# Kernel tuning notes

Hardware: AMD Instinct MI355X
Metric: run time of the kernel (lower is better)

## Reference

```python
import jax, jax.numpy as jnp
import numpy as np

L = 4
B_LIST = [30, 17, 9, 5, 3]      # bandwidth schedule (geometric 30 -> 3)
F_LIST = [1, 2, 5, 12, 28, 64]  # channel schedule (geometric 1 -> 64)
BATCH = 32
C64 = jnp.complex64

# near-identity grids (beta = pi/16, 6 alphas; SO3 grid additionally 6 gammas)
_A6 = np.linspace(0.0, 2 * np.pi, 6, endpoint=False)
S2_BETA = np.full(6, np.pi / 16)
S2_ALPHA = _A6
_aa, _gg = np.meshgrid(_A6, _A6, indexing='ij')
SO3_ALPHA = _aa.ravel()
SO3_BETA = np.full(36, np.pi / 16)
SO3_GAMMA = _gg.ravel()


def betas_of(b):
    return np.pi * (2 * np.arange(2 * b) + 1) / (4 * b)


def quad_weights(b):
    j = np.arange(2 * b)
    k = np.arange(b)
    s = (np.sin(np.pi * np.outer(2 * j + 1, 2 * k + 1) / (4 * b)) / (2 * k + 1)).sum(1)
    return (2.0 / b) * np.sin(np.pi * (2 * j + 1) / (4 * b)) * s


def wigner_d_all(lmax, betas):
    """Wigner small-d d^l_{m',m}(beta) via exp(-i beta Jy); list_l of [nbeta,2l+1,2l+1]."""
    out = [np.ones((len(betas), 1, 1))]
    for l in range(1, lmax):
        m = np.arange(-l, l)
        jp = np.sqrt(l * (l + 1) - m * (m + 1))  # <m+1|J+|m>
        Jy = np.zeros((2 * l + 1, 2 * l + 1), np.complex128)
        i = np.arange(2 * l)
        Jy[i + 1, i] = -0.5j * jp
        Jy[i, i + 1] = 0.5j * jp
        lam, U = np.linalg.eigh(Jy)
        ph = np.exp(-1j * np.outer(betas, lam))
        out.append(np.einsum('ak,bk,ck->bac', U, ph, U.conj()).real)
    return out


def fft_idx(l, n):
    # indices of frequencies m = -l..l in fft ordering of length n
    return np.concatenate([np.arange(n - l, n), np.arange(l + 1)])


def s2_fft(x, b_out):
    # x: [B,f,2b,2b] real (beta,alpha) -> list_l of [B,f,2l+1] complex
    b_in = x.shape[-1] // 2
    wig = wigner_d_all(b_out, betas_of(b_in))
    w = quad_weights(b_in)
    xf = jnp.fft.fft(x, axis=-1)
    out = []
    for l in range(b_out):
        dl = jnp.asarray((wig[l][:, :, l] * w[:, None]).astype(np.complex64))  # [2b,2l+1]
        out.append(jnp.einsum('bfjm,jm->bfm', xf[..., fft_idx(l, 2 * b_in)], dl))
    return out


def so3_fft(x, b_out):
    # x: [B,f,2b,2b,2b] real (beta,alpha,gamma) -> list_l of [B,f,2l+1,2l+1]
    b_in = x.shape[-1] // 2
    wig = wigner_d_all(b_out, betas_of(b_in))
    w = quad_weights(b_in)
    xf = jnp.fft.fft2(x, axes=(-2, -1))
    out = []
    for l in range(b_out):
        idx = fft_idx(l, 2 * b_in)
        dl = jnp.asarray((wig[l] * w[:, None, None]).astype(np.complex64))
        out.append(jnp.einsum('bfjmn,jmn->bfmn', xf[:, :, :, idx[:, None], idx[None, :]], dl))
    return out


def so3_ifft(coeffs, b):
    # coeffs: list_l [B,f,2l+1,2l+1] -> real signal [B,f,2b,2b,2b]
    wig = wigner_d_all(b, betas_of(b))
    nb = 2 * b
    Bz, f = coeffs[0].shape[:2]
    X = jnp.zeros((Bz, f, nb, nb, nb), C64)
    for l in range(b):
        idx = fft_idx(l, nb)
        dl = jnp.asarray(((2 * l + 1) * wig[l]).astype(np.complex64))
        X = X.at[:, :, :, idx[:, None], idx[None, :]].add(
            jnp.einsum('bfmn,jmn->bfjmn', coeffs[l], dl))
    return (jnp.fft.ifft2(X, axes=(-2, -1)) * (nb * nb)).real


def s2_kernel_ft(k, b):
    # k: [f_in,f_out,P] -> list_l of [2l+1,f_in,f_out] complex
    wig = wigner_d_all(b, S2_BETA)
    kc = k.astype(C64)
    out = []
    for l in range(b):
        m = np.arange(-l, l + 1)
        F = (wig[l][:, :, l] * np.exp(1j * np.outer(S2_ALPHA, m))).astype(np.complex64)
        out.append(jnp.einsum('iop,pm->mio', kc, jnp.asarray(F)))
    return out


def so3_kernel_ft(k, b):
    # k: [f_in,f_out,P] -> list_l of [2l+1,2l+1,f_in,f_out] complex
    wig = wigner_d_all(b, SO3_BETA)
    kc = k.astype(C64)
    out = []
    for l in range(b):
        m = np.arange(-l, l + 1)
        F = (wig[l]
             * np.exp(1j * np.outer(SO3_ALPHA, m))[:, :, None]
             * np.exp(1j * np.outer(SO3_GAMMA, m))[:, None, :]).astype(np.complex64)
        out.append(jnp.einsum('iop,pmn->mnio', kc, jnp.asarray(F)))
    return out


def s2_conv(x, kern, b_out):
    xh = s2_fft(x, b_out)
    kh = s2_kernel_ft(kern, b_out)
    yh = [jnp.einsum('bim,nio->bomn', xh[l], kh[l].conj()) for l in range(b_out)]
    return so3_ifft(yh, b_out)


def so3_conv(x, kern, b_out):
    xh = so3_fft(x, b_out)
    kh = so3_kernel_ft(kern, b_out)
    yh = [jnp.einsum('bimk,nkio->bomn', xh[l], kh[l].conj()) for l in range(b_out)]
    return so3_ifft(yh, b_out)


def so3_integrate(x):
    b = x.shape[-1] // 2
    w = jnp.asarray(quad_weights(b).astype(np.float32))
    return jnp.einsum('bfjac,j->bf', x, w) / float((2 * b) ** 2)


def batchnorm(x, g, be):
    mu = x.mean(0)
    var = ((x - mu) ** 2).mean(0)
    return (x - mu) * jax.lax.rsqrt(var + 1e-5) * g + be


def setup_inputs() -> dict:
    key = jax.random.key(0)
    ks = jax.random.split(key, 10)
    rn = lambda k, s, sc=1.0: jax.random.normal(k, s, jnp.float32) * sc
    return {
        'x': rn(ks[0], (BATCH, 1, 60, 60)),
        'k_s2': rn(ks[1], (1, 2, 6), 0.5),
        'k1': rn(ks[2], (2, 5, 36), 0.1),
        'k2': rn(ks[3], (5, 12, 36), 0.1),
        'k3': rn(ks[4], (12, 28, 36), 0.1),
        'k4': rn(ks[5], (28, 64, 36), 0.1),
        'g1': jnp.ones(64), 'be1': jnp.zeros(64),
        'w1': rn(ks[6], (64, 64), 0.125), 'b1': jnp.zeros(64),
        'g2': jnp.ones(64), 'be2': jnp.zeros(64),
        'w2': rn(ks[7], (64, 32), 0.125), 'b2': jnp.zeros(32),
        'g3': jnp.ones(32), 'be3': jnp.zeros(32),
        'w3': rn(ks[8], (32, 10), 0.18), 'b3': jnp.zeros(10),
    }


def reference(x, k_s2, k1, k2, k3, k4, g1, be1, w1, b1, g2, be2, w2, b2, g3, be3, w3, b3):
    h = jax.nn.relu(s2_conv(x, k_s2, B_LIST[0]))            # [B,2,60,60,60]
    for k, bo in zip((k1, k2, k3, k4), B_LIST[1:]):
        h = jax.nn.relu(so3_conv(h, k, bo))                 # bandwidth shrinks 17,9,5,3
    h = so3_integrate(h)                                    # [B,64]
    h = jax.nn.relu(batchnorm(h, g1, be1) @ w1 + b1)
    h = jax.nn.relu(batchnorm(h, g2, be2) @ w2 + b2)
    return batchnorm(h, g3, be3) @ w3 + b3                  # [B,10]
```

## Files before the change

### kernel.cpp

```cpp
#include <hip/hip_runtime.h>
#include <cmath>
#include <cstring>
#include <vector>


#define DPI 3.14159265358979323846

static constexpr int OQh(int l) { return l*(4*l*l - 1)/3; }
static_assert(OQh(30) == 35990, "oq30");
static_assert(OQh(17) == 6545,  "oq17");
static_assert(OQh(9)  == 969,   "oq9");
static_assert(OQh(5)  == 165,   "oq5");
static_assert(OQh(3)  == 35,    "oq3");

static constexpr size_t WS_XF1 = 0;
static constexpr size_t WS_XH1 = WS_XF1 + 32ull*60*30*8;
static constexpr size_t WS_KH1 = WS_XH1 + 32ull*900*8;
static constexpr size_t WS_YH1 = WS_KH1 + 1800ull*8;
static constexpr size_t WS_XT2 = WS_YH1 + 64ull*35990*8;
static constexpr size_t WS_XH2 = WS_XT2 + 64ull*60*561*8;
static constexpr size_t WS_KH2 = WS_XH2 + 64ull*6545*8;
static constexpr size_t WS_YH2 = WS_KH2 + 6545ull*10*8;
static constexpr size_t WS_XT3 = WS_YH2 + 160ull*6545*8;
static constexpr size_t WS_XH3 = WS_XT3 + 160ull*34*153*8;
static constexpr size_t WS_KH3 = WS_XH3 + 160ull*969*8;
static constexpr size_t WS_YH3 = WS_KH3 + 969ull*60*8;
static constexpr size_t WS_XT4 = WS_YH3 + 384ull*969*8;
static constexpr size_t WS_XH4 = WS_XT4 + 384ull*18*45*8;
static constexpr size_t WS_KH4 = WS_XH4 + 384ull*165*8;
static constexpr size_t WS_YH4 = WS_KH4 + 165ull*336*8;
static constexpr size_t WS_XT5 = WS_YH4 + 896ull*165*8;
static constexpr size_t WS_XH5 = WS_XT5 + 896ull*10*15*8;
static constexpr size_t WS_KH5 = WS_XH5 + 896ull*35*8;
static constexpr size_t WS_YH5 = WS_KH5 + 35ull*1792*8;
static constexpr size_t WS_S5P = WS_YH5 + 2048ull*35*8;
static constexpr size_t WS_TOTAL = WS_S5P + 2048ull*6*4;

struct ConstOffs {
  size_t A1, A2, A3, A4, A5;
  size_t S1, S2, S3, S4, S5;
  size_t WInt;
  size_t nF;
  size_t Fs2, Fso3;
  size_t Tw60, Tw34, Tw18, Tw10, Tw6;
  size_t Wn1, Wn2o, Wn3, Wn4, Wn5;
  size_t Wg1, Wg2, Wg3, Wg4;
  size_t nC;
};
static ConstOffs CO;
static float*  g_devF = nullptr;
static float2* g_devC = nullptr;

static void tqli(double* d, double* e, int n, double* z) {
  e[n-1] = 0.0;
  for (int l = 0; l < n; l++) {
    int iter = 0;
    int m;
    do {
      for (m = l; m < n-1; m++) {
        double dd = fabs(d[m]) + fabs(d[m+1]);
        if (fabs(e[m]) <= 1e-300 + 1e-14*dd) break;
      }
      if (m != l) {
        if (iter++ == 80) break;
        double g = (d[l+1]-d[l])/(2.0*e[l]);
        double r = hypot(g, 1.0);
        g = d[m]-d[l]+e[l]/(g + (g >= 0.0 ? fabs(r) : -fabs(r)));
        double s = 1.0, c = 1.0, p = 0.0;
        int i;
        r = 1.0;
        for (i = m-1; i >= l; i--) {
          double f = s*e[i], b = c*e[i];
          r = hypot(f, g);
          e[i+1] = r;
          if (r == 0.0) { d[i+1] -= p; e[m] = 0.0; break; }
          s = f/r; c = g/r;
          g = d[i+1]-p;
          r = (d[i]-g)*s + 2.0*c*b;
          p = s*r;
          d[i+1] = g+p;
          g = c*r-b;
          for (int k = 0; k < n; k++) {
            f = z[(size_t)k*n+i+1];
            z[(size_t)k*n+i+1] = s*z[(size_t)k*n+i] + c*f;
            z[(size_t)k*n+i]   = c*z[(size_t)k*n+i] - s*f;
          }
        }
        if (r == 0.0 && i >= l) continue;
        d[l] -= p; e[l] = g; e[m] = 0.0;
      }
    } while (m != l);
  }
}

struct Builder {
  std::vector<std::vector<double>> V, Lam;
  bool useExpm[30];

  Builder() {
    V.resize(30); Lam.resize(30);
    for (int l = 0; l < 30; l++) {
      int n = 2*l+1;
      std::vector<double> d(n, 0.0), e(n, 0.0), z((size_t)n*n, 0.0);
      for (int i = 0; i < n; i++) z[(size_t)i*n+i] = 1.0;
      for (int i = 0; i+1 < n; i++) {
        double m = (double)i - l;
        e[i] = -0.5*sqrt((double)l*(l+1) - m*(m+1.0));
      }
      if (n > 1) tqli(d.data(), e.data(), n, z.data());
      V[l] = std::move(z); Lam[l] = std::move(d);
    }
    std::vector<double> t((size_t)59*59);
    for (int l = 0; l < 30; l++) {
      useExpm[l] = false;
      if (l == 0) continue;
      int n = 2*l+1;
      eigD(l, 0.77, t.data());
      double corner = pow(cos(0.385), 2.0*l);
      double err = fabs(t[0] - corner) + fabs(t[(size_t)(n-1)*n + (n-1)] - corner);
      double s = 0.0;
      for (int c = 0; c < n; c++) s += t[c]*t[c];
      err += fabs(s - 1.0);
      if (!(err < 1e-8)) useExpm[l] = true;
    }
  }

  void eigD(int l, double beta, double* out) {
    int n = 2*l+1;
    const double* Vp = V[l].data();
    const double* lam = Lam[l].data();
    double ck[64], sk[64];
    for (int k = 0; k < n; k++) { ck[k] = cos(beta*lam[k]); sk[k] = sin(beta*lam[k]); }
    for (int a = 0; a < n; a++) {
      const double* va = Vp + (size_t)a*n;
      for (int c = 0; c < n; c++) {
        const double* vc = Vp + (size_t)c*n;
        int r = ((a - c) % 4 + 4) % 4;
        const double* f = (r & 1) ? sk : ck;
        double s = 0.0;
        for (int k = 0; k < n; k++) s += va[k]*vc[k]*f[k];
        out[(size_t)a*n + c] = (r >= 2) ? -s : s;
      }
    }
  }

  void expmD(int l, double beta, double* out) {
    int n = 2*l+1;
    int s = 0; double bl = fabs(beta)*(double)l + 1e-12;
    while (bl > 0.25) { bl *= 0.5; s++; }
    double sc = ldexp(beta, -s);
    std::vector<double> sup(n > 1 ? n-1 : 0);
    for (int i = 0; i+1 < n; i++) {
      double m = (double)i - l;
      sup[i] = 0.5*sqrt((double)l*(l+1) - m*(m+1.0))*sc;
    }
    std::vector<double> term((size_t)n*n, 0.0), acc((size_t)n*n, 0.0), t2((size_t)n*n);
    for (int i = 0; i < n; i++) { term[(size_t)i*n+i] = 1.0; acc[(size_t)i*n+i] = 1.0; }
    for (int k = 1; k <= 16; k++) {
      for (int r = 0; r < n; r++)
        for (int c = 0; c < n; c++) {
          double v = 0.0;
          if (c > 0)   v += term[(size_t)r*n + c-1]*sup[c-1];
          if (c+1 < n) v -= term[(size_t)r*n + c+1]*sup[c];
          t2[(size_t)r*n+c] = v/(double)k;
        }
      term.swap(t2);
      for (size_t i2 = 0; i2 < (size_t)n*n; i2++) acc[i2] += term[i2];
    }
    for (int t = 0; t < s; t++) {
      for (int r = 0; r < n; r++)
        for (int c = 0; c < n; c++) {
          double v = 0.0;
          for (int k = 0; k < n; k++) v += acc[(size_t)r*n+k]*acc[(size_t)k*n+c];
          t2[(size_t)r*n+c] = v;
        }
      acc.swap(t2);
    }
    std::memcpy(out, acc.data(), sizeof(double)*(size_t)n*n);
  }

  void buildD(int l, double beta, double* out) {
    if (useExpm[l]) expmD(l, beta, out); else eigD(l, beta, out);
  }
};

static std::vector<double> quadw_h(int b) {
  std::vector<double> w(2*b);
  for (int j = 0; j < 2*b; j++) {
    double s = 0;
    for (int k = 0; k < b; k++)
      s += sin(DPI*(2*j+1)*(2*k+1)/(4.0*b))/(double)(2*k+1);
    w[j] = (2.0/b)*sin(DPI*(2*j+1)/(4.0*b))*s;
  }
  return w;
}

static void build_all() {
  size_t o = 0;
  CO.A1 = o; o += 60ull*900;
  CO.A2 = o; o += 60ull*OQh(17);
  CO.A3 = o; o += 34ull*OQh(9);
  CO.A4 = o; o += 18ull*OQh(5);
  CO.A5 = o; o += 10ull*OQh(3);
  CO.S1 = o; o += 60ull*OQh(30);
  CO.S2 = o; o += 34ull*OQh(17);
  CO.S3 = o; o += 18ull*OQh(9);
  CO.S4 = o; o += 10ull*OQh(5);
  CO.S5 = o; o +=  6ull*OQh(3);
  CO.WInt = o; o += 8;
  CO.nF = o;
  size_t c = 0;
  CO.Fs2  = c; c += 6ull*900;
  CO.Fso3 = c; c += 36ull*OQh(17);
  CO.Tw60 = c; c += 60; CO.Tw34 = c; c += 34; CO.Tw18 = c; c += 18;
  CO.Tw10 = c; c += 10; CO.Tw6  = c; c += 6;
  CO.Wn1 = c; c += 30*60; CO.Wn2o = c; c += 17*34; CO.Wn3 = c; c += 9*18;
  CO.Wn4 = c; c += 5*10;  CO.Wn5 = c; c += 3*6;
  CO.Wg1 = c; c += 60*17; CO.Wg2 = c; c += 34*9; CO.Wg3 = c; c += 18*5;
  CO.Wg4 = c; c += 10*3;
  CO.nC = c;

  std::vector<float> HF(CO.nF, 0.f);
  std::vector<float> HC(2*CO.nC, 0.f);

  Builder B;
  auto betas = [](int b){ std::vector<double> v(2*b);
    for (int j = 0; j < 2*b; j++) v[j] = DPI*(2*j+1)/(4.0*b); return v; };
  auto w30 = quadw_h(30), w17 = quadw_h(17), w9 = quadw_h(9), w5 = quadw_h(5), w3 = quadw_h(3);
  std::vector<double> tmp((size_t)59*59);

  { auto bs = betas(30);
    for (int l = 0; l < 30; l++) { int n = 2*l+1;
      for (int j = 0; j < 60; j++) {
        B.buildD(l, bs[j], tmp.data());
        float* dst = HF.data() + CO.S1 + 60ull*OQh(l) + (size_t)j*n*n;
        for (int i2 = 0; i2 < n*n; i2++) dst[i2] = (float)((2*l+1)*tmp[i2]);
        if (l < 17) {
          float* dA = HF.data() + CO.A2 + 60ull*OQh(l) + (size_t)j*n*n;
          for (int i2 = 0; i2 < n*n; i2++) dA[i2] = (float)(tmp[i2]*w30[j]);
        }
        float* dA1 = HF.data() + CO.A1 + 60ull*l*l + (size_t)j*n;
        for (int mi = 0; mi < n; mi++) dA1[mi] = (float)(tmp[(size_t)mi*n + l]*w30[j]);
      } } }
  { auto bs = betas(17);
    for (int l = 0; l < 17; l++) { int n = 2*l+1;
      for (int j = 0; j < 34; j++) {
        B.buildD(l, bs[j], tmp.data());
        float* dst = HF.data() + CO.S2 + 34ull*OQh(l) + (size_t)j*n*n;
        for (int i2 = 0; i2 < n*n; i2++) dst[i2] = (float)((2*l+1)*tmp[i2]);
        if (l < 9) {
          float* dA = HF.data() + CO.A3 + 34ull*OQh(l) + (size_t)j*n*n;
          for (int i2 = 0; i2 < n*n; i2++) dA[i2] = (float)(tmp[i2]*w17[j]);
        } } } }
  { auto bs = betas(9);
    for (int l = 0; l < 9; l++) { int n = 2*l+1;
      for (int j = 0; j < 18; j++) {
        B.buildD(l, bs[j], tmp.data());
        float* dst = HF.data() + CO.S3 + 18ull*OQh(l) + (size_t)j*n*n;
        for (int i2 = 0; i2 < n*n; i2++) dst[i2] = (float)((2*l+1)*tmp[i2]);
        if (l < 5) {
          float* dA = HF.data() + CO.A4 + 18ull*OQh(l) + (size_t)j*n*n;
          for (int i2 = 0; i2 < n*n; i2++) dA[i2] = (float)(tmp[i2]*w9[j]);
        } } } }
  { auto bs = betas(5);
    for (int l = 0; l < 5; l++) { int n = 2*l+1;
      for (int j = 0; j < 10; j++) {
        B.buildD(l, bs[j], tmp.data());
        float* dst = HF.data() + CO.S4 + 10ull*OQh(l) + (size_t)j*n*n;
        for (int i2 = 0; i2 < n*n; i2++) dst[i2] = (float)((2*l+1)*tmp[i2]);
        if (l < 3) {
          float* dA = HF.data() + CO.A5 + 10ull*OQh(l) + (size_t)j*n*n;
          for (int i2 = 0; i2 < n*n; i2++) dA[i2] = (float)(tmp[i2]*w5[j]);
        } } } }
  { auto bs = betas(3);
    for (int l = 0; l < 3; l++) { int n = 2*l+1;
      for (int j = 0; j < 6; j++) {
        B.buildD(l, bs[j], tmp.data());
        float* dst = HF.data() + CO.S5 + 6ull*OQh(l) + (size_t)j*n*n;
        for (int i2 = 0; i2 < n*n; i2++) dst[i2] = (float)((2*l+1)*tmp[i2]);
      } } }
  { double beta = DPI/16.0;
    for (int l = 0; l < 30; l++) { int n = 2*l+1;
      B.buildD(l, beta, tmp.data());
      for (int p = 0; p < 6; p++) {
        double al = 2.0*DPI*p/6.0;
        for (int mi = 0; mi < n; mi++) {
          double ph = al*(double)(mi - l);
          double dr = tmp[(size_t)mi*n + l];
          size_t off = CO.Fs2 + 6ull*l*l + (size_t)p*n + mi;
          HC[2*off]   = (float)(dr*cos(ph));
          HC[2*off+1] = (float)(dr*sin(ph));
        } }
      if (l < 17) {
        for (int p = 0; p < 36; p++) {
          double al = 2.0*DPI*(p/6)/6.0, ga = 2.0*DPI*(p%6)/6.0;
          for (int mi = 0; mi < n; mi++)
            for (int ni = 0; ni < n; ni++) {
              double ph = al*(double)(mi - l) + ga*(double)(ni - l);
              double dr = tmp[(size_t)mi*n + ni];
              size_t off = CO.Fso3 + 36ull*OQh(l) + (size_t)p*n*n + (size_t)mi*n + ni;
              HC[2*off]   = (float)(dr*cos(ph));
              HC[2*off+1] = (float)(dr*sin(ph));
            } } } } }
  auto fillTw = [&](size_t ofs, int N){
    for (int t = 0; t < N; t++) {
      HC[2*(ofs+t)]   = (float)cos(2.0*DPI*t/N);
      HC[2*(ofs+t)+1] = (float)sin(2.0*DPI*t/N);
    } };
  fillTw(CO.Tw60, 60); fillTw(CO.Tw34, 34); fillTw(CO.Tw18, 18);
  fillTw(CO.Tw10, 10); fillTw(CO.Tw6, 6);
  auto fillWn = [&](size_t ofs, int BQ, int N){
    for (int n = 0; n < BQ; n++)
      for (int cc2 = 0; cc2 < N; cc2++) {
        double f = (n == 0) ? 1.0 : 2.0;
        HC[2*(ofs + (size_t)n*N + cc2)]   = (float)(f*cos(2.0*DPI*n*cc2/N));
        HC[2*(ofs + (size_t)n*N + cc2)+1] = (float)(f*sin(2.0*DPI*n*cc2/N));
      } };
  auto fillWg = [&](size_t ofs, int N, int KT){
    for (int cc2 = 0; cc2 < N; cc2++)
      for (int k = 0; k < KT; k++) {
        HC[2*(ofs + (size_t)cc2*KT + k)]   = (float)cos(2.0*DPI*k*cc2/N);
        HC[2*(ofs + (size_t)cc2*KT + k)+1] = (float)(-sin(2.0*DPI*k*cc2/N));
      } };
  fillWn(CO.Wn1, 30, 60); fillWn(CO.Wn2o, 17, 34); fillWn(CO.Wn3, 9, 18);
  fillWn(CO.Wn4, 5, 10);  fillWn(CO.Wn5, 3, 6);
  fillWg(CO.Wg1, 60, 17); fillWg(CO.Wg2, 34, 9); fillWg(CO.Wg3, 18, 5);
  fillWg(CO.Wg4, 10, 3);
  for (int j = 0; j < 6; j++) HF[CO.WInt + j] = (float)(w3[j]/36.0);

  size_t fb = CO.nF * sizeof(float);
  size_t fbA = (fb + 255) & ~(size_t)255;
  size_t cb = CO.nC * sizeof(float2);
  void* base = nullptr;
  if (hipMalloc(&base, fbA + cb) != hipSuccess || !base) return;
  if (hipMemcpy(base, HF.data(), fb, hipMemcpyHostToDevice) != hipSuccess) return;
  if (hipMemcpy((char*)base + fbA, HC.data(), cb, hipMemcpyHostToDevice) != hipSuccess) return;
  (void)hipDeviceSynchronize();
  g_devF = (float*)base;
  g_devC = (float2*)((char*)base + fbA);
}
namespace { struct InitOnce { InitOnce(){ build_all(); } } g_once; }

__device__ __forceinline__ int OQ(int l) { return l*(4*l*l - 1)/3; }
__device__ __forceinline__ int lFromQ(int q, int L) {
  int l = 0;
  while (l+1 < L && OQ(l+1) <= q) l++;
  return l;
}
__device__ __forceinline__ int lsq(int q) {
  int l = (int)sqrtf((float)q);
  while ((l+1)*(l+1) <= q) l++;
  while (l*l > q) l--;
  return l;
}
__device__ __forceinline__ void rotf(float2& r, float2 s) {
  float t = r.x*s.x - r.y*s.y;
  r.y = r.x*s.y + r.y*s.x;
  r.x = t;
}

__global__ __launch_bounds__(256) void k_kh_s2(
    const float* __restrict__ ks2, const float2* __restrict__ F, float2* __restrict__ kh)
{
  int id = blockIdx.x*blockDim.x + threadIdx.x;
  if (id >= 1800) return;
  int q = id >> 1, o = id & 1;
  int l = lsq(q); int W = 2*l+1; int mi = q - l*l;
  const float2* Fb = F + 6ull*l*l;
  float ax = 0.f, ay = 0.f;
  for (int p = 0; p < 6; p++) {
    float kv = ks2[o*6 + p];
    float2 f = Fb[p*W + mi];
    ax += kv*f.x; ay += kv*f.y;
  }
  kh[(size_t)q*2 + o] = make_float2(ax, ay);
}

__global__ __launch_bounds__(256) void k_kh_so3(
    const float* __restrict__ kk, const float2* __restrict__ F,
    float2* __restrict__ kh, int L, int fi, int fo)
{
  int id = blockIdx.x*blockDim.x + threadIdx.x;
  int ff = fi*fo;
  if (id >= OQ(L)*ff) return;
  int q = id / ff, r = id - q*ff;
  int i = r / fo, o = r - i*fo;
  int l = lFromQ(q, L); int W = 2*l+1; int W21 = W*W;
  int rem = q - OQ(l);
  const float2* Fb = F + 36ull*OQ(l) + rem;
  const float* kb = kk + (size_t)(i*fo + o)*36;
  float ax = 0.f, ay = 0.f;
  for (int p = 0; p < 36; p++) {
    float kv = kb[p];
    float2 f = Fb[(size_t)p*W21];
    ax += kv*f.x; ay += kv*f.y;
  }
  kh[(size_t)q*ff + r] = make_float2(ax, ay);
}

__global__ __launch_bounds__(64) void k_s1_fftA(
    const float* __restrict__ x, const float2* __restrict__ tw, float2* __restrict__ XF1)
{
  __shared__ float row[60];
  int b = blockIdx.x / 60, j = blockIdx.x - b*60;
  int t = threadIdx.x;
  if (t < 60) row[t] = x[((size_t)b*60 + j)*60 + t];
  __syncthreads();
  if (t < 30) {
    float ax = 0.f, ay = 0.f;
    int ti = 0;
    for (int a = 0; a < 60; a++) {
      float2 w = tw[ti];
      ax += row[a]*w.x; ay -= row[a]*w.y;
      ti += t; if (ti >= 60) ti -= 60;
    }
    XF1[((size_t)b*60 + j)*30 + t] = make_float2(ax, ay);
  }
}

__global__ __launch_bounds__(256) void k_s1_coef(
    const float2* __restrict__ XF1, const float* __restrict__ dA1, float2* __restrict__ xh1)
{
  int id = blockIdx.x*blockDim.x + threadIdx.x;
  if (id >= 32*900) return;
  int b = id / 900, q = id - b*900;
  int l = lsq(q); int W = 2*l+1; int mi = q - l*l; int m = mi - l;
  const float* dp = dA1 + 60ull*l*l + mi;
  const float2* xb = XF1 + (size_t)b*60*30;
  int ma = m >= 0 ? m : -m;
  float sg = m >= 0 ? 1.f : -1.f;
  float ax = 0.f, ay = 0.f;
  for (int j = 0; j < 60; j++) {
    float2 xf = xb[j*30 + ma];
    float d = dp[(size_t)j*W];
    ax += d*xf.x; ay += sg*d*xf.y;
  }
  xh1[id] = make_float2(ax, ay);
}

__global__ __launch_bounds__(256) void k_s1_yh(
    const float2* __restrict__ xh1, const float2* __restrict__ kh1, float2* __restrict__ yh1)
{
  int id = blockIdx.x*blockDim.x + threadIdx.x;
  if (id >= 64*35990) return;
  int bo = id / 35990, q = id - bo*35990;
  int b = bo >> 1, o = bo & 1;
  int l = lFromQ(q, 30); int W = 2*l+1;
  int rem = q - OQ(l); int mi = rem / W, ni = rem - mi*W;
  float2 xv = xh1[(size_t)b*900 + l*l + mi];
  float2 kv = kh1[(size_t)(l*l + ni)*2 + o];
  yh1[id] = make_float2(xv.x*kv.x + xv.y*kv.y, xv.y*kv.x - xv.x*kv.y);
}

__global__ __launch_bounds__(256) void k_yh(
    const float2* __restrict__ xh, const float2* __restrict__ kh,
    float2* __restrict__ yh, int L, int fi, int fo, int Qtot)
{
  int id = blockIdx.x*blockDim.x + threadIdx.x;
  if (id >= 32*fo*Qtot) return;
  int bo = id / Qtot, q = id - bo*Qtot;
  int b = bo / fo, o = bo - b*fo;
  int l = lFromQ(q, L); int W = 2*l+1;
  int rem = q - OQ(l); int mi = rem / W, ni = rem - mi*W;
  int ff = fi*fo;
  const float2* xb = xh + ((size_t)b*fi)*Qtot + OQ(l) + mi*W;
  const float2* kb = kh + ((size_t)(OQ(l) + ni*W))*ff + o;
  float ax = 0.f, ay = 0.f;
  for (int i = 0; i < fi; i++) {
    const float2* xrow = xb + (size_t)i*Qtot;
    const float2* krow = kb + (size_t)i*fo;
    for (int k = 0; k < W; k++) {
      float2 xv = xrow[k];
      float2 kv = krow[(size_t)k*ff];
      ax += xv.x*kv.x + xv.y*kv.y;
      ay += xv.y*kv.x - xv.x*kv.y;
    }
  }
  yh[id] = make_float2(ax, ay);
}

__global__ __launch_bounds__(256) void k_coef(
    const float2* __restrict__ xt, const float* __restrict__ dA,
    float2* __restrict__ xh, int L, int nj, int KT, int MT, int Qtot, int nbi)
{
  int id = blockIdx.x*blockDim.x + threadIdx.x;
  if (id >= nbi*Qtot) return;
  int bi = id / Qtot, q = id - bi*Qtot;
  int l = lFromQ(q, L); int W = 2*l+1; int W21 = W*W;
  int rem = q - OQ(l); int mi = rem / W, ki = rem - mi*W;
  int m = mi - l, ks = ki - l;
  const float* dAp = dA + (size_t)nj*OQ(l) + rem;
  int MTKT = MT*KT;
  int pidx; float sgn;
  if (ks >= 0) { pidx = (m + (KT-1))*KT + ks;  sgn =  1.f; }
  else         { pidx = (-m + (KT-1))*KT - ks; sgn = -1.f; }
  const float2* xb = xt + (size_t)bi*nj*MTKT + pidx;
  float ax = 0.f, ay = 0.f;
  for (int j = 0; j < nj; j++) {
    float2 xv = xb[(size_t)j*MTKT];
    float d = dAp[(size_t)j*W21];
    ax += d*xv.x; ay += sgn*d*xv.y;
  }
  xh[id] = make_float2(ax, ay);
}

template<int BQ, int N, int KT, int MT, int TPB>
__global__ __launch_bounds__(TPB) void k_synth3(
    const float2* __restrict__ yh, const float* __restrict__ dS,
    const float2* __restrict__ twN, float2* __restrict__ xt)
{
  constexpr int W2  = 2*BQ - 1;
  constexpr int NH  = N/2;
  constexpr int CP  = (BQ+3) & ~3;
  constexpr int KTP = (KT+1) & ~1;
  constexpr int QT  = BQ*(4*BQ*BQ - 1)/3;
  constexpr int R3  = (N%4 == 0) ? 4 : 2;
  constexpr int RP  = (NH%2 == 0) ? 2 : 1;
  constexpr int SZA0 = (W2*CP*8 > 2*N*NH*4) ? W2*CP*8 : 2*N*NH*4;
  constexpr int SZA  = (SZA0 + 15) & ~15;
  constexpr int SZB0 = (N*CP*8 > 2*NH*KTP*8) ? N*CP*8 : 2*NH*KTP*8;
  constexpr int SZB  = (SZB0 + 15) & ~15;
  __shared__ __align__(16) char smem[SZA + SZB + N*8];
  float2* P   = (float2*)smem;
  float*  SS  = (float*)smem;
  float*  SD  = SS + N*NH;
  float2* Tm  = (float2*)(smem + SZA);
  float2* USS = (float2*)(smem + SZA);
  float2* USD = USS + NH*KTP;
  float2* twl = (float2*)(smem + SZA + SZB);

  const int tid = threadIdx.x;
  int nwg = gridDim.x, bidx = blockIdx.x;
  int per = nwg >> 3;
  int swz = (bidx & 7)*per + (bidx >> 3);
  int bo = swz / N, j = swz - bo*N;

  for (int t = tid; t < N; t += TPB) twl[t] = twN[t];

  const float2* yhb = yh + (size_t)bo*QT;
  for (int idx = tid; idx < W2*CP; idx += TPB) {
    int pm = idx / CP, n = idx - pm*CP;
    float ax = 0.f, ay = 0.f;
    if (n < BQ) {
      int m = pm - (BQ-1);
      int am = m < 0 ? -m : m;
      int lmin = am > n ? am : n;
      int base = lmin*(4*lmin*lmin - 1)/3;
      for (int l = lmin; l < BQ; l++) {
        int Wl = 2*l+1;
        float2 y = yhb[base + (m+l)*Wl + (n+l)];
        float d = dS[(size_t)N*base + (size_t)j*Wl*Wl + (m+l)*Wl + (n+l)];
        ax += d*y.x; ay += d*y.y;
        base += Wl*Wl;
      }
    }
    P[idx] = make_float2(ax, ay);
  }
  __syncthreads();

  {
    constexpr int CG = CP/4;
    constexpr float SGN = ((BQ-1) & 1) ? -1.f : 1.f;
    const float4* P4 = (const float4*)P;
    for (int it = tid; it < NH*CG; it += TPB) {
      int a = it / CG, cg = it - a*CG;
      float2 s2 = twl[2*a];
      float2 r = make_float2(1.f, 0.f);
      float4 E0 = {0,0,0,0}, E1 = {0,0,0,0}, O0 = {0,0,0,0}, O1 = {0,0,0,0};
      for (int jj = 0; jj < BQ-1; jj++) {
        float4 e0 = P4[(2*jj)*(CP/2) + 2*cg];
        float4 e1 = P4[(2*jj)*(CP/2) + 2*cg + 1];
        float4 o0 = P4[(2*jj+1)*(CP/2) + 2*cg];
        float4 o1 = P4[(2*jj+1)*(CP/2) + 2*cg + 1];
        E0.x += e0.x*r.x - e0.y*r.y; E0.y += e0.x*r.y + e0.y*r.x;
        E0.z += e0.z*r.x - e0.w*r.y; E0.w += e0.z*r.y + e0.w*r.x;
        E1.x += e1.x*r.x - e1.y*r.y; E1.y += e1.x*r.y + e1.y*r.x;
        E1.z += e1.z*r.x - e1.w*r.y; E1.w += e1.z*r.y + e1.w*r.x;
        O0.x += o0.x*r.x - o0.y*r.y; O0.y += o0.x*r.y + o0.y*r.x;
        O0.z += o0.z*r.x - o0.w*r.y; O0.w += o0.z*r.y + o0.w*r.x;
        O1.x += o1.x*r.x - o1.y*r.y; O1.y += o1.x*r.y + o1.y*r.x;
        O1.z += o1.z*r.x - o1.w*r.y; O1.w += o1.z*r.y + o1.w*r.x;
        rotf(r, s2);
      }
      {
        float4 e0 = P4[(2*(BQ-1))*(CP/2) + 2*cg];
        float4 e1 = P4[(2*(BQ-1))*(CP/2) + 2*cg + 1];
        E0.x += e0.x*r.x - e0.y*r.y; E0.y += e0.x*r.y + e0.y*r.x;
        E0.z += e0.z*r.x - e0.w*r.y; E0.w += e0.z*r.y + e0.w*r.x;
        E1.x += e1.x*r.x - e1.y*r.y; E1.y += e1.x*r.y + e1.y*r.x;
        E1.z += e1.z*r.x - e1.w*r.y; E1.w += e1.z*r.y + e1.w*r.x;
      }
      float2 wa = twl[a];
      int pidx = (N - (a*(BQ-1)) % N) % N;
      float2 ph = twl[pidx];
      int c0 = 4*cg;
      auto doCol = [&](float ex, float ey, float ox, float oy, int col) {
        float gx = ox*wa.x - oy*wa.y, gy = ox*wa.y + oy*wa.x;
        float px = ex + gx, py = ey + gy;
        float qx = ex - gx, qy = ey - gy;
        Tm[a*CP + col]        = make_float2(px*ph.x - py*ph.y, px*ph.y + py*ph.x);
        Tm[(a+NH)*CP + col]   = make_float2(SGN*(qx*ph.x - qy*ph.y), SGN*(qx*ph.y + qy*ph.x));
      };
      doCol(E0.x, E0.y, O0.x, O0.y, c0+0);
      doCol(E0.z, E0.w, O0.z, O0.w, c0+1);
      doCol(E1.x, E1.y, O1.x, O1.y, c0+2);
      doCol(E1.z, E1.w, O1.z, O1.w, c0+3);
    }
  }
  __syncthreads();

  {
    constexpr int NO3 = BQ/2;
    constexpr int NRG = N/R3;
    for (int it = tid; it < NRG*NH; it += TPB) {
      int rg = it / NH, c = it - rg*NH;
      int a0 = rg*R3;
      float2 se = twl[2*c];
      float2 re = make_float2(1.f, 0.f);
      float2 ro = twl[c];
      float er[R3], orr[R3];
      #pragma unroll
      for (int rr = 0; rr < R3; rr++) { er[rr] = 0.f; orr[rr] = 0.f; }
      for (int jj = 0; jj < NO3; jj++) {
        #pragma unroll
        for (int rr = 0; rr < R3; rr++) {
          float4 tv = *(const float4*)&Tm[(a0+rr)*CP + 2*jj];
          er[rr]  += tv.x*re.x - tv.y*re.y;
          orr[rr] += tv.z*ro.x - tv.w*ro.y;
        }
        rotf(re, se); rotf(ro, se);
      }
      if constexpr ((BQ & 1) != 0) {
        #pragma unroll
        for (int rr = 0; rr < R3; rr++) {
          float2 tv = Tm[(a0+rr)*CP + (BQ-1)];
          er[rr] += tv.x*re.x - tv.y*re.y;
        }
      }
      #pragma unroll
      for (int rr = 0; rr < R3; rr++) {
        float t0x = Tm[(a0+rr)*CP].x;
        float s0 = fmaxf(2.f*(er[rr] + orr[rr]) - t0x, 0.f);
        float s1 = fmaxf(2.f*(er[rr] - orr[rr]) - t0x, 0.f);
        SS[(a0+rr)*NH + c] = s0 + s1;
        SD[(a0+rr)*NH + c] = s0 - s1;
      }
    }
  }
  __syncthreads();

  {
    for (int it = tid; it < (NH/RP)*KT; it += TPB) {
      int g = it / KT, k = it - g*KT;
      int a0 = g*RP;
      const float* Sp = (k & 1) ? SD : SS;
      float2 st = twl[k]; st.y = -st.y;
      float2 r = make_float2(1.f, 0.f);
      float ux[2*RP], uy[2*RP];
      #pragma unroll
      for (int q2 = 0; q2 < 2*RP; q2++) { ux[q2] = 0.f; uy[q2] = 0.f; }
      for (int c = 0; c < NH; c++) {
        #pragma unroll
        for (int pp = 0; pp < RP; pp++) {
          float sl = Sp[(a0+pp)*NH + c];
          float sh = Sp[(a0+pp+NH)*NH + c];
          ux[2*pp]   += sl*r.x; uy[2*pp]   += sl*r.y;
          ux[2*pp+1] += sh*r.x; uy[2*pp+1] += sh*r.y;
        }
        rotf(r, st);
      }
      #pragma unroll
      for (int pp = 0; pp < RP; pp++) {
        USS[(a0+pp)*KTP + k] = make_float2(ux[2*pp] + ux[2*pp+1], uy[2*pp] + uy[2*pp+1]);
        USD[(a0+pp)*KTP + k] = make_float2(ux[2*pp] - ux[2*pp+1], uy[2*pp] - uy[2*pp+1]);
      }
    }
  }
  __syncthreads();

  {
    float2* xtb = xt + ((size_t)bo*N + j)*(MT*KT);
    constexpr int KG = KTP/2;
    for (int it = tid; it < MT*KG; it += TPB) {
      int pm2 = it / KG, kg = it - pm2*KG;
      int m = pm2 - (KT-1);
      int mm = m < 0 ? m + N : m;
      const float2* Up = (m & 1) ? USD : USS;
      float2 st = twl[mm];
      float2 r = make_float2(1.f, 0.f);
      float a0x = 0.f, a0y = 0.f, a1x = 0.f, a1y = 0.f;
      for (int a = 0; a < NH; a++) {
        float4 u = *(const float4*)&Up[a*KTP + 2*kg];
        a0x += u.x*r.x + u.y*r.y;  a0y += u.y*r.x - u.x*r.y;
        a1x += u.z*r.x + u.w*r.y;  a1y += u.w*r.x - u.z*r.y;
        rotf(r, st);
      }
      int k0 = 2*kg;
      xtb[pm2*KT + k0] = make_float2(a0x, a0y);
      if (k0 + 1 < KT) xtb[pm2*KT + k0 + 1] = make_float2(a1x, a1y);
    }
  }
}

template<int BQ, int N, int KT, int MT, int INTEG, int NPAIR, int TPB>
__global__ __launch_bounds__(TPB) void k_synth2(
    const float2* __restrict__ yh, const float* __restrict__ dS,
    const float2* __restrict__ twN, const float2* __restrict__ Wn2,
    const float2* __restrict__ Wg, float2* __restrict__ xt,
    float* __restrict__ s5p, const float* __restrict__ wInt)
{
  constexpr int W2 = 2*BQ - 1;
  constexpr int QT = BQ*(4*BQ*BQ - 1)/3;
  constexpr int SZA = (((W2*BQ*8 > N*N*4) ? W2*BQ*8 : N*N*4) + 15) & ~15;
  constexpr int SZB0 = (N*BQ*8 > N*KT*8) ? N*BQ*8 : N*KT*8;
  constexpr int SZB1 = (SZB0 > TPB*4) ? SZB0 : TPB*4;
  constexpr int SZB = (SZB1 + 15) & ~15;
  __shared__ __align__(16) char smem[SZA + SZB + N*8];
  float2* P   = (float2*)smem;
  float*  S   = (float*)smem;
  float2* Tm  = (float2*)(smem + SZA);
  float2* U   = (float2*)(smem + SZA);
  float*  red = (float*)(smem + SZA);
  float2* twl = (float2*)(smem + SZA + SZB);

  const int tid = threadIdx.x;
  int bidx = blockIdx.x, nwg = gridDim.x;
  int per = nwg >> 3;
  int swz = (bidx & 7)*per + (bidx >> 3);
  int bo = swz / N, j = swz - bo*N;

  for (int t = tid; t < N; t += TPB) twl[t] = twN[t];
  __syncthreads();

  const float2* yhb = yh + (size_t)bo*QT;
  for (int idx = tid; idx < W2*BQ; idx += TPB) {
    int pm = idx / BQ, n = idx - pm*BQ;
    int m = pm - (BQ-1);
    int am = m < 0 ? -m : m;
    int lmin = am > n ? am : n;
    int base = lmin*(4*lmin*lmin - 1)/3;
    float ax = 0.f, ay = 0.f;
    for (int l = lmin; l < BQ; l++) {
      int Wl = 2*l+1;
      float2 y = yhb[base + (m+l)*Wl + (n+l)];
      float d = dS[(size_t)N*base + (size_t)j*Wl*Wl + (m+l)*Wl + (n+l)];
      ax += d*y.x; ay += d*y.y;
      base += Wl*Wl;
    }
    P[idx] = make_float2(ax, ay);
  }
  __syncthreads();

  for (int idx = tid; idx < (N/2)*BQ; idx += TPB) {
    int ag = idx / BQ, n = idx - ag*BQ;
    int a0 = 2*ag, a1 = a0 + 1;
    int t0 = (N - (a0*(BQ-1)) % N) % N;
    int t1 = (N - (a1*(BQ-1)) % N) % N;
    float2 A0 = {0,0}, A1 = {0,0};
    for (int pm = 0; pm < W2; pm++) {
      float2 p = P[pm*BQ + n];
      float2 w0 = twl[t0], w1 = twl[t1];
      A0.x += p.x*w0.x - p.y*w0.y; A0.y += p.x*w0.y + p.y*w0.x;
      A1.x += p.x*w1.x - p.y*w1.y; A1.y += p.x*w1.y + p.y*w1.x;
      t0 += a0; if (t0 >= N) t0 -= N;
      t1 += a1; if (t1 >= N) t1 -= N;
    }
    Tm[a0*BQ + n] = A0;
    Tm[a1*BQ + n] = A1;
  }
  __syncthreads();

  {
    constexpr int CG = N/2;
    const float4* WnR = (const float4*)Wn2;
    for (int idx = tid; idx < N*CG; idx += TPB) {
      int a = idx / CG, cg = idx - a*CG;
      float s0 = 0.f, s1 = 0.f;
      const float2* TmA = Tm + a*BQ;
      for (int n = 0; n < BQ; n++) {
        float2 T = TmA[n];
        float4 w = WnR[n*CG + cg];
        s0 += T.x*w.x - T.y*w.y;
        s1 += T.x*w.z - T.y*w.w;
      }
      s0 = fmaxf(s0, 0.f); s1 = fmaxf(s1, 0.f);
      *(float2*)&S[a*N + 2*cg] = make_float2(s0, s1);
    }
  }
  __syncthreads();

  if constexpr (!INTEG) {
    for (int idx = tid; idx < (N/2)*KT; idx += TPB) {
      int ag = idx / KT, k = idx - ag*KT;
      int a0 = 2*ag, a1 = a0 + 1;
      float u0x=0.f,u0y=0.f,u1x=0.f,u1y=0.f;
      const float* S0 = S + a0*N;
      const float* S1 = S + a1*N;
      for (int c = 0; c < N; c++) {
        float2 w = Wg[c*KT + k];
        u0x += S0[c]*w.x; u0y += S0[c]*w.y;
        u1x += S1[c]*w.x; u1y += S1[c]*w.y;
      }
      U[a0*KT + k] = make_float2(u0x, u0y);
      U[a1*KT + k] = make_float2(u1x, u1y);
    }
    __syncthreads();

    float2* xtb = xt + ((size_t)bo*N + j)*(MT*KT);
    for (int idx = tid; idx < MT*KT; idx += TPB) {
      int pm2 = idx / KT, k = idx - pm2*KT;
      int m = pm2 - (KT-1);
      float ax = 0.f, ay = 0.f;
      int t = 0;
      for (int a = 0; a < N; a++) {
        float2 u = U[a*KT + k];
        float2 w = twl[t];
        ax += u.x*w.x + u.y*w.y;
        ay += u.y*w.x - u.x*w.y;
        t += m; if (t < 0) t += N; else if (t >= N) t -= N;
      }
      xtb[idx] = make_float2(ax, ay);
    }
  } else {
    float part = 0.f;
    for (int idx = tid; idx < N*N; idx += TPB) part += S[idx];
    red[tid] = part;
    __syncthreads();
    for (int off2 = TPB >> 1; off2 > 0; off2 >>= 1) {
      if (tid < off2) red[tid] += red[tid + off2];
      __syncthreads();
    }
    if (tid == 0) s5p[bo*N + j] = red[0]*wInt[j];
  }
}

__global__ __launch_bounds__(256) void k_mlp(
    const float* __restrict__ s5p,
    const float* __restrict__ g1, const float* __restrict__ be1,
    const float* __restrict__ w1, const float* __restrict__ b1,
    const float* __restrict__ g2, const float* __restrict__ be2,
    const float* __restrict__ w2, const float* __restrict__ b2,
    const float* __restrict__ g3, const float* __restrict__ be3,
    const float* __restrict__ w3, const float* __restrict__ b3,
    float* __restrict__ out)
{
  __shared__ float A[2048], Bs[2048], C[1024], mu[64], iv[64];
  int tid = threadIdx.x;
  for (int idx = tid; idx < 2048; idx += 256) {
    float s = 0.f;
    #pragma unroll
    for (int j = 0; j < 6; j++) s += s5p[idx*6 + j];
    A[idx] = s;
  }
  __syncthreads();
  if (tid < 64) {
    float m = 0.f; for (int b = 0; b < 32; b++) m += A[b*64 + tid]; m *= (1.f/32);
    float v = 0.f; for (int b = 0; b < 32; b++) { float d = A[b*64+tid]-m; v += d*d; } v *= (1.f/32);
    mu[tid] = m; iv[tid] = rsqrtf(v + 1e-5f)*g1[tid];
  }
  __syncthreads();
  for (int idx = tid; idx < 2048; idx += 256) {
    int f = idx & 63;
    A[idx] = (A[idx]-mu[f])*iv[f] + be1[f];
  }
  __syncthreads();
  for (int idx = tid; idx < 2048; idx += 256) {
    int b = idx >> 6, fo = idx & 63;
    float s = b1[fo];
    for (int f = 0; f < 64; f++) s += A[b*64+f]*w1[f*64+fo];
    Bs[idx] = fmaxf(s, 0.f);
  }
  __syncthreads();
  if (tid < 64) {
    float m = 0.f; for (int b = 0; b < 32; b++) m += Bs[b*64+tid]; m *= (1.f/32);
    float v = 0.f; for (int b = 0; b < 32; b++) { float d = Bs[b*64+tid]-m; v += d*d; } v *= (1.f/32);
    mu[tid] = m; iv[tid] = rsqrtf(v + 1e-5f)*g2[tid];
  }
  __syncthreads();
  for (int idx = tid; idx < 2048; idx += 256) {
    int f = idx & 63;
    Bs[idx] = (Bs[idx]-mu[f])*iv[f] + be2[f];
  }
  __syncthreads();
  for (int idx = tid; idx < 1024; idx += 256) {
    int b = idx >> 5, fo = idx & 31;
    float s = b2[fo];
    for (int f = 0; f < 64; f++) s += Bs[b*64+f]*w2[f*32+fo];
    C[idx] = fmaxf(s, 0.f);
  }
  __syncthreads();
  if (tid < 32) {
    float m = 0.f; for (int b = 0; b < 32; b++) m += C[b*32+tid]; m *= (1.f/32);
    float v = 0.f; for (int b = 0; b < 32; b++) { float d = C[b*32+tid]-m; v += d*d; } v *= (1.f/32);
    mu[tid] = m; iv[tid] = rsqrtf(v + 1e-5f)*g3[tid];
  }
  __syncthreads();
  for (int idx = tid; idx < 1024; idx += 256) {
    int f = idx & 31;
    C[idx] = (C[idx]-mu[f])*iv[f] + be3[f];
  }
  __syncthreads();
  for (int idx = tid; idx < 320; idx += 256) {
    int b = idx/10, cc = idx - b*10;
    float s = b3[cc];
    for (int f = 0; f < 32; f++) s += C[b*32+f]*w3[f*10+cc];
    out[idx] = s;
  }
}

static inline int cdiv_h(int a, int b) { return (a + b - 1)/b; }

extern "C" void kernel_launch(void* const* d_in, const int* in_sizes, int n_in,
                              void* d_out, int out_size, void* d_ws, size_t ws_size,
                              hipStream_t stream) {
  (void)in_sizes; (void)n_in; (void)out_size;
  if (!g_devF || !g_devC || ws_size < WS_TOTAL) return;

  const float* x    = (const float*)d_in[0];
  const float* ks2  = (const float*)d_in[1];
  const float* k1   = (const float*)d_in[2];
  const float* k2   = (const float*)d_in[3];
  const float* k3   = (const float*)d_in[4];
  const float* k4   = (const float*)d_in[5];
  const float* g1   = (const float*)d_in[6],  *be1 = (const float*)d_in[7];
  const float* w1   = (const float*)d_in[8],  *b1  = (const float*)d_in[9];
  const float* g2   = (const float*)d_in[10], *be2 = (const float*)d_in[11];
  const float* w2   = (const float*)d_in[12], *b2  = (const float*)d_in[13];
  const float* g3   = (const float*)d_in[14], *be3 = (const float*)d_in[15];
  const float* w3   = (const float*)d_in[16], *b3  = (const float*)d_in[17];
  float* out = (float*)d_out;
  char* ws = (char*)d_ws;

  float2* XF1 = (float2*)(ws + WS_XF1);
  float2* xh1 = (float2*)(ws + WS_XH1);
  float2* kh1 = (float2*)(ws + WS_KH1);
  float2* yh1 = (float2*)(ws + WS_YH1);
  float2* xt2 = (float2*)(ws + WS_XT2);
  float2* xh2 = (float2*)(ws + WS_XH2);
  float2* kh2 = (float2*)(ws + WS_KH2);
  float2* yh2 = (float2*)(ws + WS_YH2);
  float2* xt3 = (float2*)(ws + WS_XT3);
  float2* xh3 = (float2*)(ws + WS_XH3);
  float2* kh3 = (float2*)(ws + WS_KH3);
  float2* yh3 = (float2*)(ws + WS_YH3);
  float2* xt4 = (float2*)(ws + WS_XT4);
  float2* xh4 = (float2*)(ws + WS_XH4);
  float2* kh4 = (float2*)(ws + WS_KH4);
  float2* yh4 = (float2*)(ws + WS_YH4);
  float2* xt5 = (float2*)(ws + WS_XT5);
  float2* xh5 = (float2*)(ws + WS_XH5);
  float2* kh5 = (float2*)(ws + WS_KH5);
  float2* yh5 = (float2*)(ws + WS_YH5);
  float*  s5p = (float*) (ws + WS_S5P);

  const float* dA1p = g_devF + CO.A1; const float* dA2p = g_devF + CO.A2;
  const float* dA3p = g_devF + CO.A3; const float* dA4p = g_devF + CO.A4;
  const float* dA5p = g_devF + CO.A5;
  const float* dS1p = g_devF + CO.S1; const float* dS2p = g_devF + CO.S2;
  const float* dS3p = g_devF + CO.S3; const float* dS4p = g_devF + CO.S4;
  const float* dS5p = g_devF + CO.S5;
  const float* wIntp = g_devF + CO.WInt;
  const float2* Fs2p  = g_devC + CO.Fs2;
  const float2* Fso3p = g_devC + CO.Fso3;
  const float2* tw60p = g_devC + CO.Tw60; const float2* tw34p = g_devC + CO.Tw34;
  const float2* tw18p = g_devC + CO.Tw18; const float2* tw10p = g_devC + CO.Tw10;
  const float2* tw6p  = g_devC + CO.Tw6;
  const float2* Wn4p = g_devC + CO.Wn4; const float2* Wn5p = g_devC + CO.Wn5;
  const float2* Wg4p = g_devC + CO.Wg4;

  constexpr int Q30 = OQh(30), Q17 = OQh(17), Q9 = OQh(9), Q5 = OQh(5), Q3 = OQh(3);

  k_kh_s2 <<<cdiv_h(1800,256),      256, 0, stream>>>(ks2, Fs2p,  kh1);
  k_kh_so3<<<cdiv_h(Q17*10,256),    256, 0, stream>>>(k1, Fso3p, kh2, 17, 2, 5);
  k_kh_so3<<<cdiv_h(Q9*60,256),     256, 0, stream>>>(k2, Fso3p, kh3, 9, 5, 12);
  k_kh_so3<<<cdiv_h(Q5*336,256),    256, 0, stream>>>(k3, Fso3p, kh4, 5, 12, 28);
  k_kh_so3<<<cdiv_h(Q3*1792,256),   256, 0, stream>>>(k4, Fso3p, kh5, 3, 28, 64);

  k_s1_fftA<<<32*60, 64, 0, stream>>>(x, tw60p, XF1);
  k_s1_coef<<<cdiv_h(32*900,256), 256, 0, stream>>>(XF1, dA1p, xh1);
  k_s1_yh  <<<cdiv_h(64*Q30,256), 256, 0, stream>>>(xh1, kh1, yh1);

  k_synth3<30,60,17,33,256><<<64*60,  256, 0, stream>>>(yh1, dS1p, tw60p, xt2);
  k_coef <<<cdiv_h(64*Q17,256),  256, 0, stream>>>(xt2, dA2p, xh2, 17, 60, 17, 33, Q17, 64);
  k_yh   <<<cdiv_h(160*Q17,256), 256, 0, stream>>>(xh2, kh2, yh2, 17, 2, 5, Q17);

  k_synth3<17,34,9,17,128><<<160*34, 128, 0, stream>>>(yh2, dS2p, tw34p, xt3);
  k_coef <<<cdiv_h(160*Q9,256),  256, 0, stream>>>(xt3, dA3p, xh3, 9, 34, 9, 17, Q9, 160);
  k_yh   <<<cdiv_h(384*Q9,256),  256, 0, stream>>>(xh3, kh3, yh3, 9, 5, 12, Q9);

  k_synth3<9,18,5,9,64><<<384*18, 64, 0, stream>>>(yh3, dS3p, tw18p, xt4);
  k_coef <<<cdiv_h(384*Q5,256),  256, 0, stream>>>(xt4, dA4p, xh4, 5, 18, 5, 9, Q5, 384);
  k_yh   <<<cdiv_h(896*Q5,256),  256, 0, stream>>>(xh4, kh4, yh4, 5, 12, 28, Q5);

  k_synth2<5,10,3,5,0,1,64><<<896*10, 64, 0, stream>>>(yh4, dS4p, tw10p, Wn4p, Wg4p, xt5, nullptr, nullptr);
  k_coef <<<cdiv_h(896*Q3,256),  256, 0, stream>>>(xt5, dA5p, xh5, 3, 10, 3, 5, Q3, 896);
  k_yh   <<<cdiv_h(2048*Q3,256), 256, 0, stream>>>(xh5, kh5, yh5, 3, 28, 64, Q3);

  k_synth2<3,6,3,5,1,1,64><<<2048*6, 64, 0, stream>>>(yh5, dS5p, tw6p, Wn5p, nullptr, nullptr, s5p, wIntp);

  k_mlp<<<1, 256, 0, stream>>>(s5p, g1, be1, w1, b1, g2, be2, w2, b2, g3, be3, w3, b3, out);
}
```

Measured before the change: 936.4 us.

## Restructure SO(3) inverse transforms into scatter plus staged DFT GEMM passes

Replaces the fused per-beta synthesis kernels for the two largest SO(3) stages with a scatter kernel that exploits Wigner-d symmetry (only n>=0 terms, packed per (m,n) with precomputed offsets), followed by separable DFT passes over alpha and gamma done as small matrix products in chunks. The spectral intermediates are transposed so batch/channel is innermost, which gives coalesced access, and the forward coefficient kernels read transposed beta-major Wigner tables and use the Hermitian half-spectrum. This is meant to cut the redundant work and uncoalesced reads in the large synthesis steps. In exchange it adds more launches and large scratch buffers, and the index bookkeeping is more intricate.

```diff
diff --git a/kernel.cpp b/kernel.cpp
--- a/kernel.cpp
+++ b/kernel.cpp
@@ -2,6 +2,7 @@
 #include <cmath>
 #include <cstring>
 #include <vector>
+#include <algorithm>
 
 
 #define DPI 3.14159265358979323846
@@ -13,43 +14,52 @@
 static_assert(OQh(5)  == 165,   "oq5");
 static_assert(OQh(3)  == 35,    "oq3");
 
-static constexpr size_t WS_XF1 = 0;
-static constexpr size_t WS_XH1 = WS_XF1 + 32ull*60*30*8;
-static constexpr size_t WS_KH1 = WS_XH1 + 32ull*900*8;
-static constexpr size_t WS_YH1 = WS_KH1 + 1800ull*8;
-static constexpr size_t WS_XT2 = WS_YH1 + 64ull*35990*8;
-static constexpr size_t WS_XH2 = WS_XT2 + 64ull*60*561*8;
-static constexpr size_t WS_KH2 = WS_XH2 + 64ull*6545*8;
-static constexpr size_t WS_YH2 = WS_KH2 + 6545ull*10*8;
-static constexpr size_t WS_XT3 = WS_YH2 + 160ull*6545*8;
-static constexpr size_t WS_XH3 = WS_XT3 + 160ull*34*153*8;
-static constexpr size_t WS_KH3 = WS_XH3 + 160ull*969*8;
-static constexpr size_t WS_YH3 = WS_KH3 + 969ull*60*8;
-static constexpr size_t WS_XT4 = WS_YH3 + 384ull*969*8;
-static constexpr size_t WS_XH4 = WS_XT4 + 384ull*18*45*8;
-static constexpr size_t WS_KH4 = WS_XH4 + 384ull*165*8;
-static constexpr size_t WS_YH4 = WS_KH4 + 165ull*336*8;
-static constexpr size_t WS_XT5 = WS_YH4 + 896ull*165*8;
-static constexpr size_t WS_XH5 = WS_XT5 + 896ull*10*15*8;
-static constexpr size_t WS_KH5 = WS_XH5 + 896ull*35*8;
-static constexpr size_t WS_YH5 = WS_KH5 + 35ull*1792*8;
-static constexpr size_t WS_S5P = WS_YH5 + 2048ull*35*8;
-static constexpr size_t WS_TOTAL = WS_S5P + 2048ull*6*4;
+static constexpr int T1SUM = 18445;
+static constexpr int T2SUM = 3417;
+
+static constexpr size_t al256(size_t x){ return (x + 255) & ~(size_t)255; }
+static constexpr size_t WS_XF1  = 0;
+static constexpr size_t WS_XH1  = WS_XF1  + al256(32ull*60*30*8);
+static constexpr size_t WS_KH1  = WS_XH1  + al256(32ull*900*8);
+static constexpr size_t WS_YH1T = WS_KH1  + al256(1800ull*8);
+static constexpr size_t WS_XH2  = WS_YH1T + al256(35990ull*64*8);
+static constexpr size_t WS_KH2  = WS_XH2  + al256(64ull*6545*8);
+static constexpr size_t WS_YH2T = WS_KH2  + al256(6545ull*10*8);
+static constexpr size_t WS_XH3  = WS_YH2T + al256(6545ull*160*8);
+static constexpr size_t WS_KH3  = WS_XH3  + al256(160ull*969*8);
+static constexpr size_t WS_YH3T = WS_KH3  + al256(969ull*60*8);
+static constexpr size_t WS_XT4  = WS_YH3T + al256(969ull*384*8);
+static constexpr size_t WS_XH4  = WS_XT4  + al256(384ull*18*45*8);
+static constexpr size_t WS_KH4  = WS_XH4  + al256(384ull*165*8);
+static constexpr size_t WS_YH4T = WS_KH4  + al256(165ull*336*8);
+static constexpr size_t WS_XT5  = WS_YH4T + al256(165ull*896*8);
+static constexpr size_t WS_XH5  = WS_XT5  + al256(896ull*10*15*8);
+static constexpr size_t WS_KH5  = WS_XH5  + al256(896ull*35*8);
+static constexpr size_t WS_YH5T = WS_KH5  + al256(35ull*1792*8);
+static constexpr size_t WS_S5P  = WS_YH5T + al256(35ull*2048*8);
+static constexpr size_t WS_XT2  = WS_S5P  + al256(2048ull*6*4);
+static constexpr size_t WS_XT3  = WS_XT2  + al256(561ull*3840*8);
+static constexpr size_t WS_RX   = WS_XT3  + al256(153ull*5440*8);
+static constexpr size_t WS_RY   = WS_RX   + al256(1770ull*960*8);
+static constexpr size_t WS_TOTAL= WS_RY   + al256(1728000ull*8);
 
 struct ConstOffs {
-  size_t A1, A2, A3, A4, A5;
-  size_t S1, S2, S3, S4, S5;
+  size_t A1, dAT2, dAT3, A4, A5;
+  size_t dT1, dT2;
+  size_t S3, S4, S5;
   size_t WInt;
   size_t nF;
   size_t Fs2, Fso3;
-  size_t Tw60, Tw34, Tw18, Tw10, Tw6;
-  size_t Wn1, Wn2o, Wn3, Wn4, Wn5;
-  size_t Wg1, Wg2, Wg3, Wg4;
+  size_t Tw60, Tw18, Tw10, Tw6;
+  size_t Wn1, Wn2o, Wn4, Wn5;
+  size_t Wg1, Wg2, Wg4;
+  size_t WA1t, WA2t, WC1, WC2;
   size_t nC;
 };
 static ConstOffs CO;
 static float*  g_devF = nullptr;
 static float2* g_devC = nullptr;
+static int*    g_devI = nullptr;
 
 static void tqli(double* d, double* e, int n, double* z) {
   e[n-1] = 0.0;
@@ -197,31 +207,47 @@
 
 static void build_all() {
   size_t o = 0;
-  CO.A1 = o; o += 60ull*900;
-  CO.A2 = o; o += 60ull*OQh(17);
-  CO.A3 = o; o += 34ull*OQh(9);
-  CO.A4 = o; o += 18ull*OQh(5);
-  CO.A5 = o; o += 10ull*OQh(3);
-  CO.S1 = o; o += 60ull*OQh(30);
-  CO.S2 = o; o += 34ull*OQh(17);
-  CO.S3 = o; o += 18ull*OQh(9);
-  CO.S4 = o; o += 10ull*OQh(5);
-  CO.S5 = o; o +=  6ull*OQh(3);
+  CO.A1   = o; o += 60ull*900;
+  CO.dAT2 = o; o += (size_t)OQh(17)*60;
+  CO.dAT3 = o; o += (size_t)OQh(9)*34;
+  CO.A4   = o; o += 18ull*OQh(5);
+  CO.A5   = o; o += 10ull*OQh(3);
+  CO.dT1  = o; o += (size_t)T1SUM*60;
+  CO.dT2  = o; o += (size_t)T2SUM*34;
+  CO.S3   = o; o += 18ull*OQh(9);
+  CO.S4   = o; o += 10ull*OQh(5);
+  CO.S5   = o; o +=  6ull*OQh(3);
   CO.WInt = o; o += 8;
   CO.nF = o;
   size_t c = 0;
   CO.Fs2  = c; c += 6ull*900;
   CO.Fso3 = c; c += 36ull*OQh(17);
-  CO.Tw60 = c; c += 60; CO.Tw34 = c; c += 34; CO.Tw18 = c; c += 18;
-  CO.Tw10 = c; c += 10; CO.Tw6  = c; c += 6;
-  CO.Wn1 = c; c += 30*60; CO.Wn2o = c; c += 17*34; CO.Wn3 = c; c += 9*18;
-  CO.Wn4 = c; c += 5*10;  CO.Wn5 = c; c += 3*6;
-  CO.Wg1 = c; c += 60*17; CO.Wg2 = c; c += 34*9; CO.Wg3 = c; c += 18*5;
-  CO.Wg4 = c; c += 10*3;
+  CO.Tw60 = c; c += 60; CO.Tw18 = c; c += 18; CO.Tw10 = c; c += 10; CO.Tw6 = c; c += 6;
+  CO.Wn1  = c; c += 30*60; CO.Wn2o = c; c += 17*34;
+  CO.Wn4  = c; c += 5*10;  CO.Wn5  = c; c += 3*6;
+  CO.Wg1  = c; c += 60*17; CO.Wg2  = c; c += 34*9; CO.Wg4 = c; c += 10*3;
+  CO.WA1t = c; c += 59*60;
+  CO.WA2t = c; c += 33*34;
+  CO.WC1  = c; c += 33*60;
+  CO.WC2  = c; c += 17*34;
   CO.nC = c;
 
   std::vector<float> HF(CO.nF, 0.f);
   std::vector<float> HC(2*CO.nC, 0.f);
+
+  std::vector<int> HI(1770 + 561);
+  { int acc = 0;
+    for (int pm = 0; pm < 59; pm++) for (int n = 0; n < 30; n++) {
+      int m = pm - 29, am = m < 0 ? -m : m;
+      int lm = am > n ? am : n;
+      HI[pm*30 + n] = acc; acc += 30 - lm;
+    } }
+  { int acc = 0;
+    for (int pm = 0; pm < 33; pm++) for (int n = 0; n < 17; n++) {
+      int m = pm - 16, am = m < 0 ? -m : m;
+      int lm = am > n ? am : n;
+      HI[1770 + pm*17 + n] = acc; acc += 17 - lm;
+    } }
 
   Builder B;
   auto betas = [](int b){ std::vector<double> v(2*b);
@@ -230,54 +256,66 @@
   std::vector<double> tmp((size_t)59*59);
 
   { auto bs = betas(30);
-    for (int l = 0; l < 30; l++) { int n = 2*l+1;
+    for (int l = 0; l < 30; l++) { int W = 2*l+1;
       for (int j = 0; j < 60; j++) {
         B.buildD(l, bs[j], tmp.data());
-        float* dst = HF.data() + CO.S1 + 60ull*OQh(l) + (size_t)j*n*n;
-        for (int i2 = 0; i2 < n*n; i2++) dst[i2] = (float)((2*l+1)*tmp[i2]);
+        for (int mm = -l; mm <= l; mm++)
+          for (int nn = 0; nn <= l; nn++) {
+            int am = mm < 0 ? -mm : mm;
+            int lmin = am > nn ? am : nn;
+            int term = HI[(mm+29)*30 + nn] + (l - lmin);
+            HF[CO.dT1 + (size_t)term*60 + j] =
+              (float)((2*l+1)*tmp[(size_t)(mm+l)*W + (nn+l)]);
+          }
         if (l < 17) {
-          float* dA = HF.data() + CO.A2 + 60ull*OQh(l) + (size_t)j*n*n;
-          for (int i2 = 0; i2 < n*n; i2++) dA[i2] = (float)(tmp[i2]*w30[j]);
+          for (int rem = 0; rem < W*W; rem++)
+            HF[CO.dAT2 + (size_t)(OQh(l)+rem)*60 + j] = (float)(tmp[rem]*w30[j]);
         }
-        float* dA1 = HF.data() + CO.A1 + 60ull*l*l + (size_t)j*n;
-        for (int mi = 0; mi < n; mi++) dA1[mi] = (float)(tmp[(size_t)mi*n + l]*w30[j]);
+        float* dA1 = HF.data() + CO.A1 + 60ull*l*l + (size_t)j*W;
+        for (int mi = 0; mi < W; mi++) dA1[mi] = (float)(tmp[(size_t)mi*W + l]*w30[j]);
       } } }
   { auto bs = betas(17);
-    for (int l = 0; l < 17; l++) { int n = 2*l+1;
+    for (int l = 0; l < 17; l++) { int W = 2*l+1;
       for (int j = 0; j < 34; j++) {
         B.buildD(l, bs[j], tmp.data());
-        float* dst = HF.data() + CO.S2 + 34ull*OQh(l) + (size_t)j*n*n;
-        for (int i2 = 0; i2 < n*n; i2++) dst[i2] = (float)((2*l+1)*tmp[i2]);
+        for (int mm = -l; mm <= l; mm++)
+          for (int nn = 0; nn <= l; nn++) {
+            int am = mm < 0 ? -mm : mm;
+            int lmin = am > nn ? am : nn;
+            int term = HI[1770 + (mm+16)*17 + nn] + (l - lmin);
+            HF[CO.dT2 + (size_t)term*34 + j] =
+              (float)((2*l+1)*tmp[(size_t)(mm+l)*W + (nn+l)]);
+          }
         if (l < 9) {
-          float* dA = HF.data() + CO.A3 + 34ull*OQh(l) + (size_t)j*n*n;
-          for (int i2 = 0; i2 < n*n; i2++) dA[i2] = (float)(tmp[i2]*w17[j]);
+          for (int rem = 0; rem < W*W; rem++)
+            HF[CO.dAT3 + (size_t)(OQh(l)+rem)*34 + j] = (float)(tmp[rem]*w17[j]);
         } } } }
   { auto bs = betas(9);
-    for (int l = 0; l < 9; l++) { int n = 2*l+1;
+    for (int l = 0; l < 9; l++) { int W = 2*l+1;
       for (int j = 0; j < 18; j++) {
         B.buildD(l, bs[j], tmp.data());
-        float* dst = HF.data() + CO.S3 + 18ull*OQh(l) + (size_t)j*n*n;
-        for (int i2 = 0; i2 < n*n; i2++) dst[i2] = (float)((2*l+1)*tmp[i2]);
+        float* dst = HF.data() + CO.S3 + 18ull*OQh(l) + (size_t)j*W*W;
+        for (int i2 = 0; i2 < W*W; i2++) dst[i2] = (float)((2*l+1)*tmp[i2]);
         if (l < 5) {
-          float* dA = HF.data() + CO.A4 + 18ull*OQh(l) + (size_t)j*n*n;
-          for (int i2 = 0; i2 < n*n; i2++) dA[i2] = (float)(tmp[i2]*w9[j]);
+          float* dA = HF.data() + CO.A4 + 18ull*OQh(l) + (size_t)j*W*W;
+          for (int i2 = 0; i2 < W*W; i2++) dA[i2] = (float)(tmp[i2]*w9[j]);
         } } } }
   { auto bs = betas(5);
-    for (int l = 0; l < 5; l++) { int n = 2*l+1;
+    for (int l = 0; l < 5; l++) { int W = 2*l+1;
       for (int j = 0; j < 10; j++) {
         B.buildD(l, bs[j], tmp.data());
-        float* dst = HF.data() + CO.S4 + 10ull*OQh(l) + (size_t)j*n*n;
-        for (int i2 = 0; i2 < n*n; i2++) dst[i2] = (float)((2*l+1)*tmp[i2]);
+        float* dst = HF.data() + CO.S4 + 10ull*OQh(l) + (size_t)j*W*W;
+        for (int i2 = 0; i2 < W*W; i2++) dst[i2] = (float)((2*l+1)*tmp[i2]);
         if (l < 3) {
-          float* dA = HF.data() + CO.A5 + 10ull*OQh(l) + (size_t)j*n*n;
-          for (int i2 = 0; i2 < n*n; i2++) dA[i2] = (float)(tmp[i2]*w5[j]);
+          float* dA = HF.data() + CO.A5 + 10ull*OQh(l) + (size_t)j*W*W;
+          for (int i2 = 0; i2 < W*W; i2++) dA[i2] = (float)(tmp[i2]*w5[j]);
         } } } }
   { auto bs = betas(3);
-    for (int l = 0; l < 3; l++) { int n = 2*l+1;
+    for (int l = 0; l < 3; l++) { int W = 2*l+1;
       for (int j = 0; j < 6; j++) {
         B.buildD(l, bs[j], tmp.data());
-        float* dst = HF.data() + CO.S5 + 6ull*OQh(l) + (size_t)j*n*n;
-        for (int i2 = 0; i2 < n*n; i2++) dst[i2] = (float)((2*l+1)*tmp[i2]);
+        float* dst = HF.data() + CO.S5 + 6ull*OQh(l) + (size_t)j*W*W;
+        for (int i2 = 0; i2 < W*W; i2++) dst[i2] = (float)((2*l+1)*tmp[i2]);
       } } }
   { double beta = DPI/16.0;
     for (int l = 0; l < 30; l++) { int n = 2*l+1;
@@ -307,8 +345,7 @@
       HC[2*(ofs+t)]   = (float)cos(2.0*DPI*t/N);
       HC[2*(ofs+t)+1] = (float)sin(2.0*DPI*t/N);
     } };
-  fillTw(CO.Tw60, 60); fillTw(CO.Tw34, 34); fillTw(CO.Tw18, 18);
-  fillTw(CO.Tw10, 10); fillTw(CO.Tw6, 6);
+  fillTw(CO.Tw60, 60); fillTw(CO.Tw18, 18); fillTw(CO.Tw10, 10); fillTw(CO.Tw6, 6);
   auto fillWn = [&](size_t ofs, int BQ, int N){
     for (int n = 0; n < BQ; n++)
       for (int cc2 = 0; cc2 < N; cc2++) {
@@ -322,22 +359,49 @@
         HC[2*(ofs + (size_t)cc2*KT + k)]   = (float)cos(2.0*DPI*k*cc2/N);
         HC[2*(ofs + (size_t)cc2*KT + k)+1] = (float)(-sin(2.0*DPI*k*cc2/N));
       } };
-  fillWn(CO.Wn1, 30, 60); fillWn(CO.Wn2o, 17, 34); fillWn(CO.Wn3, 9, 18);
+  fillWn(CO.Wn1, 30, 60); fillWn(CO.Wn2o, 17, 34);
   fillWn(CO.Wn4, 5, 10);  fillWn(CO.Wn5, 3, 6);
-  fillWg(CO.Wg1, 60, 17); fillWg(CO.Wg2, 34, 9); fillWg(CO.Wg3, 18, 5);
-  fillWg(CO.Wg4, 10, 3);
+  fillWg(CO.Wg1, 60, 17); fillWg(CO.Wg2, 34, 9); fillWg(CO.Wg4, 10, 3);
+  for (int pm = 0; pm < 59; pm++)
+    for (int a = 0; a < 60; a++) {
+      double th = 2.0*DPI*a*(pm-29)/60.0;
+      HC[2*(CO.WA1t + (size_t)pm*60 + a)]   = (float)cos(th);
+      HC[2*(CO.WA1t + (size_t)pm*60 + a)+1] = (float)sin(th);
+    }
+  for (int pm = 0; pm < 33; pm++)
+    for (int a = 0; a < 34; a++) {
+      double th = 2.0*DPI*a*(pm-16)/34.0;
+      HC[2*(CO.WA2t + (size_t)pm*34 + a)]   = (float)cos(th);
+      HC[2*(CO.WA2t + (size_t)pm*34 + a)+1] = (float)sin(th);
+    }
+  for (int p = 0; p < 33; p++)
+    for (int a = 0; a < 60; a++) {
+      double th = 2.0*DPI*(p-16)*a/60.0;
+      HC[2*(CO.WC1 + (size_t)p*60 + a)]   = (float)cos(th);
+      HC[2*(CO.WC1 + (size_t)p*60 + a)+1] = (float)sin(th);
+    }
+  for (int p = 0; p < 17; p++)
+    for (int a = 0; a < 34; a++) {
+      double th = 2.0*DPI*(p-8)*a/34.0;
+      HC[2*(CO.WC2 + (size_t)p*34 + a)]   = (float)cos(th);
+      HC[2*(CO.WC2 + (size_t)p*34 + a)+1] = (float)sin(th);
+    }
   for (int j = 0; j < 6; j++) HF[CO.WInt + j] = (float)(w3[j]/36.0);
 
-  size_t fb = CO.nF * sizeof(float);
-  size_t fbA = (fb + 255) & ~(size_t)255;
-  size_t cb = CO.nC * sizeof(float2);
+  size_t fb  = CO.nF * sizeof(float);
+  size_t fbA = al256(fb);
+  size_t cb  = CO.nC * sizeof(float2);
+  size_t cbA = al256(cb);
+  size_t ib  = HI.size() * sizeof(int);
   void* base = nullptr;
-  if (hipMalloc(&base, fbA + cb) != hipSuccess || !base) return;
+  if (hipMalloc(&base, fbA + cbA + ib) != hipSuccess || !base) return;
   if (hipMemcpy(base, HF.data(), fb, hipMemcpyHostToDevice) != hipSuccess) return;
   if (hipMemcpy((char*)base + fbA, HC.data(), cb, hipMemcpyHostToDevice) != hipSuccess) return;
+  if (hipMemcpy((char*)base + fbA + cbA, HI.data(), ib, hipMemcpyHostToDevice) != hipSuccess) return;
   (void)hipDeviceSynchronize();
   g_devF = (float*)base;
   g_devC = (float2*)((char*)base + fbA);
+  g_devI = (int*)((char*)base + fbA + cbA);
 }
 namespace { struct InitOnce { InitOnce(){ build_all(); } } g_once; }
 
@@ -438,27 +502,28 @@
   xh1[id] = make_float2(ax, ay);
 }
 
-__global__ __launch_bounds__(256) void k_s1_yh(
-    const float2* __restrict__ xh1, const float2* __restrict__ kh1, float2* __restrict__ yh1)
-{
-  int id = blockIdx.x*blockDim.x + threadIdx.x;
-  if (id >= 64*35990) return;
-  int bo = id / 35990, q = id - bo*35990;
+__global__ __launch_bounds__(256) void k_s1_yh_t(
+    const float2* __restrict__ xh1, const float2* __restrict__ kh1, float2* __restrict__ yht)
+{
+  int id = blockIdx.x*256 + threadIdx.x;
+  if (id >= 35990*64) return;
+  int q = id >> 6, bo = id & 63;
   int b = bo >> 1, o = bo & 1;
   int l = lFromQ(q, 30); int W = 2*l+1;
   int rem = q - OQ(l); int mi = rem / W, ni = rem - mi*W;
   float2 xv = xh1[(size_t)b*900 + l*l + mi];
   float2 kv = kh1[(size_t)(l*l + ni)*2 + o];
-  yh1[id] = make_float2(xv.x*kv.x + xv.y*kv.y, xv.y*kv.x - xv.x*kv.y);
-}
-
-__global__ __launch_bounds__(256) void k_yh(
+  yht[id] = make_float2(xv.x*kv.x + xv.y*kv.y, xv.y*kv.x - xv.x*kv.y);
+}
+
+__global__ __launch_bounds__(256) void k_yh_t(
     const float2* __restrict__ xh, const float2* __restrict__ kh,
-    float2* __restrict__ yh, int L, int fi, int fo, int Qtot)
-{
-  int id = blockIdx.x*blockDim.x + threadIdx.x;
-  if (id >= 32*fo*Qtot) return;
-  int bo = id / Qtot, q = id - bo*Qtot;
+    float2* __restrict__ yht, int L, int fi, int fo, int Qtot)
+{
+  int id = blockIdx.x*256 + threadIdx.x;
+  int BOF = 32*fo;
+  if (id >= Qtot*BOF) return;
+  int q = id / BOF, bo = id - q*BOF;
   int b = bo / fo, o = bo - b*fo;
   int l = lFromQ(q, L); int W = 2*l+1;
   int rem = q - OQ(l); int mi = rem / W, ni = rem - mi*W;
@@ -476,7 +541,34 @@
       ay += xv.y*kv.x - xv.x*kv.y;
     }
   }
-  yh[id] = make_float2(ax, ay);
+  yht[id] = make_float2(ax, ay);
+}
+
+template<int L, int NJ, int KT, int TPB>
+__global__ __launch_bounds__(TPB) void k_coef_t(
+    const float2* __restrict__ xtN, const float* __restrict__ dAT,
+    float2* __restrict__ xh, int Qtot, int nbi, int SLfull)
+{
+  int id = blockIdx.x*TPB + threadIdx.x;
+  if (id >= nbi*Qtot) return;
+  int bi = id / Qtot, q = id - bi*Qtot;
+  int l = lFromQ(q, L); int W = 2*l+1;
+  int rem = q - OQ(l); int mi = rem / W, ki = rem - mi*W;
+  int m = mi - l, ks = ki - l;
+  int pidx; float sgn;
+  if (ks >= 0) { pidx = (m + (KT-1))*KT + ks;  sgn =  1.f; }
+  else         { pidx = (-m + (KT-1))*KT - ks; sgn = -1.f; }
+  const float2* xb = xtN + (size_t)pidx*SLfull + (size_t)bi*NJ;
+  const float* dp = dAT + (size_t)q*NJ;
+  float ax = 0.f, ay = 0.f;
+  #pragma unroll 4
+  for (int j = 0; j < NJ; j += 2) {
+    float2 d2 = *(const float2*)&dp[j];
+    float2 xa = xb[j], xc = xb[j+1];
+    ax += d2.x*xa.x + d2.y*xc.x;
+    ay += d2.x*xa.y + d2.y*xc.y;
+  }
+  xh[id] = make_float2(ax, sgn*ay);
 }
 
 __global__ __launch_bounds__(256) void k_coef(
@@ -504,7 +596,158 @@
   xh[id] = make_float2(ax, ay);
 }
 
-template<int BQ, int N, int KT, int MT, int TPB>
+
+template<int BQ, int NJ, int BOC, int TPB>
+__global__ __launch_bounds__(TPB) void k_scat(
+    const float2* __restrict__ yht, const float* __restrict__ dT,
+    const int* __restrict__ toff, float2* __restrict__ P,
+    int boLo, int BO)
+{
+  constexpr int CH = BOC*NJ;
+  __shared__ float2 Ys[BQ*BOC];
+  __shared__ float  Ds[BQ*NJ];
+  const int mn = blockIdx.x;
+  const int pm = mn / BQ, n = mn - pm*BQ;
+  const int m = pm - (BQ-1);
+  const int am = m < 0 ? -m : m;
+  const int lmin = am > n ? am : n;
+  const int K = BQ - lmin;
+  const int tof = toff[mn];
+  for (int idx = threadIdx.x; idx < K*BOC; idx += TPB) {
+    int kk = idx / BOC, bo = idx - kk*BOC;
+    int l = lmin + kk;
+    int q = OQ(l) + (m+l)*(2*l+1) + (n+l);
+    Ys[idx] = yht[(size_t)q*BO + boLo + bo];
+  }
+  for (int idx = threadIdx.x; idx < K*NJ; idx += TPB)
+    Ds[idx] = dT[(size_t)tof*NJ + idx];
+  __syncthreads();
+  float2* Pb = P + (size_t)mn*CH;
+  for (int o = threadIdx.x; o < CH; o += TPB) {
+    int bo = o / NJ, j = o - bo*NJ;
+    float ax = 0.f, ay = 0.f;
+    for (int kk = 0; kk < K; kk++) {
+      float2 y = Ys[kk*BOC + bo];
+      float d = Ds[kk*NJ + j];
+      ax = fmaf(d, y.x, ax); ay = fmaf(d, y.y, ay);
+    }
+    Pb[o] = make_float2(ax, ay);
+  }
+}
+
+template<int NPM, int NN, int AROWS, int NAH, int NAT, int CHSL, int TPB>
+__global__ __launch_bounds__(TPB) void k_dftA(
+    const float2* __restrict__ P, const float2* __restrict__ WA,
+    float2* __restrict__ Tm)
+{
+  constexpr int SLT = (CHSL + TPB - 1)/TPB;
+  __shared__ float2 Wl[NPM*AROWS];
+  int b = blockIdx.x;
+  int t = b % SLT; int rest = b / SLT;
+  int ah = rest % NAH; int n = rest / NAH;
+  int aBase = ah*AROWS;
+  for (int i = threadIdx.x; i < NPM*AROWS; i += TPB) {
+    int pm = i / AROWS, al = i - pm*AROWS;
+    Wl[i] = WA[(size_t)pm*NAT + aBase + al];
+  }
+  __syncthreads();
+  int sl = t*TPB + threadIdx.x;
+  if (sl >= CHSL) return;
+  float2 acc[AROWS];
+  #pragma unroll
+  for (int a = 0; a < AROWS; a++) acc[a] = make_float2(0.f, 0.f);
+  for (int pm = 0; pm < NPM; pm++) {
+    float2 p = P[((size_t)pm*NN + n)*CHSL + sl];
+    const float2* wr = &Wl[pm*AROWS];
+    #pragma unroll
+    for (int a = 0; a < AROWS; a++) {
+      float2 w = wr[a];
+      acc[a].x = fmaf(p.x, w.x, fmaf(-p.y, w.y, acc[a].x));
+      acc[a].y = fmaf(p.x, w.y, fmaf( p.y, w.x, acc[a].y));
+    }
+  }
+  #pragma unroll
+  for (int a = 0; a < AROWS; a++)
+    Tm[((size_t)(aBase + a)*NN + n)*CHSL + sl] = acc[a];
+}
+
+template<int NN, int NC, int KT, int CHSL, int TPB>
+__global__ __launch_bounds__(TPB) void k_dftB(
+    const float2* __restrict__ Tm, const float2* __restrict__ Wn,
+    const float2* __restrict__ Wg, float2* __restrict__ U)
+{
+  constexpr int SLT = (CHSL + TPB - 1)/TPB;
+  __shared__ float2 WnL[NN*NC];
+  __shared__ float2 WgT[KT*NC];
+  int b = blockIdx.x;
+  int t = b % SLT; int a = b / SLT;
+  for (int i = threadIdx.x; i < NN*NC; i += TPB) WnL[i] = Wn[i];
+  for (int i = threadIdx.x; i < KT*NC; i += TPB) {
+    int k = i / NC, c = i - k*NC;
+    WgT[i] = Wg[(size_t)c*KT + k];
+  }
+  __syncthreads();
+  int sl = t*TPB + threadIdx.x;
+  if (sl >= CHSL) return;
+  float S[NC];
+  #pragma unroll
+  for (int c = 0; c < NC; c++) S[c] = 0.f;
+  for (int n = 0; n < NN; n++) {
+    float2 tv = Tm[((size_t)a*NN + n)*CHSL + sl];
+    const float2* wr = &WnL[n*NC];
+    #pragma unroll
+    for (int c = 0; c < NC; c++)
+      S[c] = fmaf(tv.x, wr[c].x, fmaf(-tv.y, wr[c].y, S[c]));
+  }
+  #pragma unroll
+  for (int c = 0; c < NC; c++) S[c] = fmaxf(S[c], 0.f);
+  for (int k = 0; k < KT; k++) {
+    const float2* wr = &WgT[k*NC];
+    float ux = 0.f, uy = 0.f;
+    #pragma unroll
+    for (int c = 0; c < NC; c++) {
+      ux = fmaf(S[c], wr[c].x, ux);
+      uy = fmaf(S[c], wr[c].y, uy);
+    }
+    U[((size_t)a*KT + k)*CHSL + sl] = make_float2(ux, uy);
+  }
+}
+
+template<int MT, int KT, int NA, int CHSL, int TPB>
+__global__ __launch_bounds__(TPB) void k_dftC(
+    const float2* __restrict__ U, const float2* __restrict__ WC,
+    float2* __restrict__ xt, int slOff, int SLfull)
+{
+  constexpr int SLT = (CHSL + TPB - 1)/TPB;
+  __shared__ float2 WcT[NA*MT];
+  int b = blockIdx.x;
+  int t = b % SLT; int k = b / SLT;
+  for (int i = threadIdx.x; i < NA*MT; i += TPB) {
+    int aa = i / MT, p = i - aa*MT;
+    WcT[i] = WC[(size_t)p*NA + aa];
+  }
+  __syncthreads();
+  int sl = t*TPB + threadIdx.x;
+  if (sl >= CHSL) return;
+  float2 acc[MT];
+  #pragma unroll
+  for (int p = 0; p < MT; p++) acc[p] = make_float2(0.f, 0.f);
+  for (int aa = 0; aa < NA; aa++) {
+    float2 u = U[((size_t)aa*KT + k)*CHSL + sl];
+    const float2* wr = &WcT[aa*MT];
+    #pragma unroll
+    for (int p = 0; p < MT; p++) {
+      float2 w = wr[p];
+      acc[p].x = fmaf(u.x, w.x, fmaf( u.y, w.y, acc[p].x));
+      acc[p].y = fmaf(u.y, w.x, fmaf(-u.x, w.y, acc[p].y));
+    }
+  }
+  #pragma unroll
+  for (int p = 0; p < MT; p++)
+    xt[((size_t)(p*KT + k))*SLfull + slOff + sl] = acc[p];
+}
+
+template<int BQ, int N, int KT, int MT, int TPB, int BO>
 __global__ __launch_bounds__(TPB) void k_synth3(
     const float2* __restrict__ yh, const float* __restrict__ dS,
     const float2* __restrict__ twN, float2* __restrict__ xt)
@@ -513,7 +756,6 @@
   constexpr int NH  = N/2;
   constexpr int CP  = (BQ+3) & ~3;
   constexpr int KTP = (KT+1) & ~1;
-  constexpr int QT  = BQ*(4*BQ*BQ - 1)/3;
   constexpr int R3  = (N%4 == 0) ? 4 : 2;
   constexpr int RP  = (NH%2 == 0) ? 2 : 1;
   constexpr int SZA0 = (W2*CP*8 > 2*N*NH*4) ? W2*CP*8 : 2*N*NH*4;
@@ -537,7 +779,6 @@
 
   for (int t = tid; t < N; t += TPB) twl[t] = twN[t];
 
-  const float2* yhb = yh + (size_t)bo*QT;
   for (int idx = tid; idx < W2*CP; idx += TPB) {
     int pm = idx / CP, n = idx - pm*CP;
     float ax = 0.f, ay = 0.f;
@@ -548,7 +789,8 @@
       int base = lmin*(4*lmin*lmin - 1)/3;
       for (int l = lmin; l < BQ; l++) {
         int Wl = 2*l+1;
-        float2 y = yhb[base + (m+l)*Wl + (n+l)];
+        int e = base + (m+l)*Wl + (n+l);
+        float2 y = yh[(size_t)e*BO + bo];
         float d = dS[(size_t)N*base + (size_t)j*Wl*Wl + (m+l)*Wl + (n+l)];
         ax += d*y.x; ay += d*y.y;
         base += Wl*Wl;
@@ -702,7 +944,7 @@
   }
 }
 
-template<int BQ, int N, int KT, int MT, int INTEG, int NPAIR, int TPB>
+template<int BQ, int N, int KT, int MT, int INTEG, int NPAIR, int TPB, int BO>
 __global__ __launch_bounds__(TPB) void k_synth2(
     const float2* __restrict__ yh, const float* __restrict__ dS,
     const float2* __restrict__ twN, const float2* __restrict__ Wn2,
@@ -710,7 +952,6 @@
     float* __restrict__ s5p, const float* __restrict__ wInt)
 {
   constexpr int W2 = 2*BQ - 1;
-  constexpr int QT = BQ*(4*BQ*BQ - 1)/3;
   constexpr int SZA = (((W2*BQ*8 > N*N*4) ? W2*BQ*8 : N*N*4) + 15) & ~15;
   constexpr int SZB0 = (N*BQ*8 > N*KT*8) ? N*BQ*8 : N*KT*8;
   constexpr int SZB1 = (SZB0 > TPB*4) ? SZB0 : TPB*4;
@@ -732,7 +973,6 @@
   for (int t = tid; t < N; t += TPB) twl[t] = twN[t];
   __syncthreads();
 
-  const float2* yhb = yh + (size_t)bo*QT;
   for (int idx = tid; idx < W2*BQ; idx += TPB) {
     int pm = idx / BQ, n = idx - pm*BQ;
     int m = pm - (BQ-1);
@@ -742,7 +982,8 @@
     float ax = 0.f, ay = 0.f;
     for (int l = lmin; l < BQ; l++) {
       int Wl = 2*l+1;
-      float2 y = yhb[base + (m+l)*Wl + (n+l)];
+      int e = base + (m+l)*Wl + (n+l);
+      float2 y = yh[(size_t)e*BO + bo];
       float d = dS[(size_t)N*base + (size_t)j*Wl*Wl + (m+l)*Wl + (n+l)];
       ax += d*y.x; ay += d*y.y;
       base += Wl*Wl;
@@ -914,7 +1155,7 @@
                               void* d_out, int out_size, void* d_ws, size_t ws_size,
                               hipStream_t stream) {
   (void)in_sizes; (void)n_in; (void)out_size;
-  if (!g_devF || !g_devC || ws_size < WS_TOTAL) return;
+  if (!g_devF || !g_devC || !g_devI || ws_size < WS_TOTAL) return;
 
   const float* x    = (const float*)d_in[0];
   const float* ks2  = (const float*)d_in[1];
@@ -931,72 +1172,102 @@
   float* out = (float*)d_out;
   char* ws = (char*)d_ws;
 
-  float2* XF1 = (float2*)(ws + WS_XF1);
-  float2* xh1 = (float2*)(ws + WS_XH1);
-  float2* kh1 = (float2*)(ws + WS_KH1);
-  float2* yh1 = (float2*)(ws + WS_YH1);
-  float2* xt2 = (float2*)(ws + WS_XT2);
-  float2* xh2 = (float2*)(ws + WS_XH2);
-  float2* kh2 = (float2*)(ws + WS_KH2);
-  float2* yh2 = (float2*)(ws + WS_YH2);
-  float2* xt3 = (float2*)(ws + WS_XT3);
-  float2* xh3 = (float2*)(ws + WS_XH3);
-  float2* kh3 = (float2*)(ws + WS_KH3);
-  float2* yh3 = (float2*)(ws + WS_YH3);
-  float2* xt4 = (float2*)(ws + WS_XT4);
-  float2* xh4 = (float2*)(ws + WS_XH4);
-  float2* kh4 = (float2*)(ws + WS_KH4);
-  float2* yh4 = (float2*)(ws + WS_YH4);
-  float2* xt5 = (float2*)(ws + WS_XT5);
-  float2* xh5 = (float2*)(ws + WS_XH5);
-  float2* kh5 = (float2*)(ws + WS_KH5);
-  float2* yh5 = (float2*)(ws + WS_YH5);
-  float*  s5p = (float*) (ws + WS_S5P);
-
-  const float* dA1p = g_devF + CO.A1; const float* dA2p = g_devF + CO.A2;
-  const float* dA3p = g_devF + CO.A3; const float* dA4p = g_devF + CO.A4;
-  const float* dA5p = g_devF + CO.A5;
-  const float* dS1p = g_devF + CO.S1; const float* dS2p = g_devF + CO.S2;
-  const float* dS3p = g_devF + CO.S3; const float* dS4p = g_devF + CO.S4;
-  const float* dS5p = g_devF + CO.S5;
+  float2* XF1  = (float2*)(ws + WS_XF1);
+  float2* xh1  = (float2*)(ws + WS_XH1);
+  float2* kh1  = (float2*)(ws + WS_KH1);
+  float2* yh1t = (float2*)(ws + WS_YH1T);
+  float2* xh2  = (float2*)(ws + WS_XH2);
+  float2* kh2  = (float2*)(ws + WS_KH2);
+  float2* yh2t = (float2*)(ws + WS_YH2T);
+  float2* xh3  = (float2*)(ws + WS_XH3);
+  float2* kh3  = (float2*)(ws + WS_KH3);
+  float2* yh3t = (float2*)(ws + WS_YH3T);
+  float2* xt4  = (float2*)(ws + WS_XT4);
+  float2* xh4  = (float2*)(ws + WS_XH4);
+  float2* kh4  = (float2*)(ws + WS_KH4);
+  float2* yh4t = (float2*)(ws + WS_YH4T);
+  float2* xt5  = (float2*)(ws + WS_XT5);
+  float2* xh5  = (float2*)(ws + WS_XH5);
+  float2* kh5  = (float2*)(ws + WS_KH5);
+  float2* yh5t = (float2*)(ws + WS_YH5T);
+  float*  s5p  = (float*) (ws + WS_S5P);
+  float2* xt2  = (float2*)(ws + WS_XT2);
+  float2* xt3  = (float2*)(ws + WS_XT3);
+  float2* RX   = (float2*)(ws + WS_RX);
+  float2* RY   = (float2*)(ws + WS_RY);
+
+  const float* dA1p  = g_devF + CO.A1;
+  const float* dAT2p = g_devF + CO.dAT2;
+  const float* dAT3p = g_devF + CO.dAT3;
+  const float* dA4p  = g_devF + CO.A4;
+  const float* dA5p  = g_devF + CO.A5;
+  const float* dT1p  = g_devF + CO.dT1;
+  const float* dT2p  = g_devF + CO.dT2;
+  const float* dS3p  = g_devF + CO.S3;
+  const float* dS4p  = g_devF + CO.S4;
+  const float* dS5p  = g_devF + CO.S5;
   const float* wIntp = g_devF + CO.WInt;
   const float2* Fs2p  = g_devC + CO.Fs2;
   const float2* Fso3p = g_devC + CO.Fso3;
-  const float2* tw60p = g_devC + CO.Tw60; const float2* tw34p = g_devC + CO.Tw34;
-  const float2* tw18p = g_devC + CO.Tw18; const float2* tw10p = g_devC + CO.Tw10;
+  const float2* tw60p = g_devC + CO.Tw60;
+  const float2* tw18p = g_devC + CO.Tw18;
+  const float2* tw10p = g_devC + CO.Tw10;
   const float2* tw6p  = g_devC + CO.Tw6;
-  const float2* Wn4p = g_devC + CO.Wn4; const float2* Wn5p = g_devC + CO.Wn5;
-  const float2* Wg4p = g_devC + CO.Wg4;
+  const float2* Wn1p  = g_devC + CO.Wn1;
+  const float2* Wn2p  = g_devC + CO.Wn2o;
+  const float2* Wn4p  = g_devC + CO.Wn4;
+  const float2* Wn5p  = g_devC + CO.Wn5;
+  const float2* Wg1p  = g_devC + CO.Wg1;
+  const float2* Wg2p  = g_devC + CO.Wg2;
+  const float2* Wg4p  = g_devC + CO.Wg4;
+  const float2* WA1p  = g_devC + CO.WA1t;
+  const float2* WA2p  = g_devC + CO.WA2t;
+  const float2* WC1p  = g_devC + CO.WC1;
+  const float2* WC2p  = g_devC + CO.WC2;
+  const int* toff1p = g_devI;
+  const int* toff2p = g_devI + 1770;
 
   constexpr int Q30 = OQh(30), Q17 = OQh(17), Q9 = OQh(9), Q5 = OQh(5), Q3 = OQh(3);
 
-  k_kh_s2 <<<cdiv_h(1800,256),      256, 0, stream>>>(ks2, Fs2p,  kh1);
-  k_kh_so3<<<cdiv_h(Q17*10,256),    256, 0, stream>>>(k1, Fso3p, kh2, 17, 2, 5);
-  k_kh_so3<<<cdiv_h(Q9*60,256),     256, 0, stream>>>(k2, Fso3p, kh3, 9, 5, 12);
-  k_kh_so3<<<cdiv_h(Q5*336,256),    256, 0, stream>>>(k3, Fso3p, kh4, 5, 12, 28);
-  k_kh_so3<<<cdiv_h(Q3*1792,256),   256, 0, stream>>>(k4, Fso3p, kh5, 3, 28, 64);
+  k_kh_s2 <<<cdiv_h(1800,256),    256, 0, stream>>>(ks2, Fs2p,  kh1);
+  k_kh_so3<<<cdiv_h(Q17*10,256),  256, 0, stream>>>(k1, Fso3p, kh2, 17, 2, 5);
+  k_kh_so3<<<cdiv_h(Q9*60,256),   256, 0, stream>>>(k2, Fso3p, kh3, 9, 5, 12);
+  k_kh_so3<<<cdiv_h(Q5*336,256),  256, 0, stream>>>(k3, Fso3p, kh4, 5, 12, 28);
+  k_kh_so3<<<cdiv_h(Q3*1792,256), 256, 0, stream>>>(k4, Fso3p, kh5, 3, 28, 64);
 
   k_s1_fftA<<<32*60, 64, 0, stream>>>(x, tw60p, XF1);
   k_s1_coef<<<cdiv_h(32*900,256), 256, 0, stream>>>(XF1, dA1p, xh1);
-  k_s1_yh  <<<cdiv_h(64*Q30,256), 256, 0, stream>>>(xh1, kh1, yh1);
-
-  k_synth3<30,60,17,33,256><<<64*60,  256, 0, stream>>>(yh1, dS1p, tw60p, xt2);
-  k_coef <<<cdiv_h(64*Q17,256),  256, 0, stream>>>(xt2, dA2p, xh2, 17, 60, 17, 33, Q17, 64);
-  k_yh   <<<cdiv_h(160*Q17,256), 256, 0, stream>>>(xh2, kh2, yh2, 17, 2, 5, Q17);
-
-  k_synth3<17,34,9,17,128><<<160*34, 128, 0, stream>>>(yh2, dS2p, tw34p, xt3);
-  k_coef <<<cdiv_h(160*Q9,256),  256, 0, stream>>>(xt3, dA3p, xh3, 9, 34, 9, 17, Q9, 160);
-  k_yh   <<<cdiv_h(384*Q9,256),  256, 0, stream>>>(xh3, kh3, yh3, 9, 5, 12, Q9);
-
-  k_synth3<9,18,5,9,64><<<384*18, 64, 0, stream>>>(yh3, dS3p, tw18p, xt4);
-  k_coef <<<cdiv_h(384*Q5,256),  256, 0, stream>>>(xt4, dA4p, xh4, 5, 18, 5, 9, Q5, 384);
-  k_yh   <<<cdiv_h(896*Q5,256),  256, 0, stream>>>(xh4, kh4, yh4, 5, 12, 28, Q5);
-
-  k_synth2<5,10,3,5,0,1,64><<<896*10, 64, 0, stream>>>(yh4, dS4p, tw10p, Wn4p, Wg4p, xt5, nullptr, nullptr);
-  k_coef <<<cdiv_h(896*Q3,256),  256, 0, stream>>>(xt5, dA5p, xh5, 3, 10, 3, 5, Q3, 896);
-  k_yh   <<<cdiv_h(2048*Q3,256), 256, 0, stream>>>(xh5, kh5, yh5, 3, 28, 64, Q3);
-
-  k_synth2<3,6,3,5,1,1,64><<<2048*6, 64, 0, stream>>>(yh5, dS5p, tw6p, Wn5p, nullptr, nullptr, s5p, wIntp);
+  k_s1_yh_t<<<cdiv_h(64*Q30,256), 256, 0, stream>>>(xh1, kh1, yh1t);
+
+  for (int c = 0; c < 4; c++) {
+    int slOff = c*960;
+    k_scat<30,60,16,256><<<1770, 256, 0, stream>>>(yh1t, dT1p, toff1p, RX, c*16, 64);
+    k_dftA<59,30,30,2,60,960,256><<<240, 256, 0, stream>>>(RX, WA1p, RY);
+    k_dftB<30,60,17,960,256><<<240, 256, 0, stream>>>(RY, Wn1p, Wg1p, RX);
+    k_dftC<33,17,60,960,256><<<68, 256, 0, stream>>>(RX, WC1p, xt2, slOff, 3840);
+  }
+  k_coef_t<17,60,17,256><<<cdiv_h(64*Q17,256), 256, 0, stream>>>(xt2, dAT2p, xh2, Q17, 64, 3840);
+  k_yh_t<<<cdiv_h(Q17*160,256), 256, 0, stream>>>(xh2, kh2, yh2t, 17, 2, 5, Q17);
+
+  for (int c = 0; c < 2; c++) {
+    int slOff = c*2720;
+    k_scat<17,34,80,256><<<561, 256, 0, stream>>>(yh2t, dT2p, toff2p, RX, c*80, 160);
+    k_dftA<33,17,34,1,34,2720,256><<<187, 256, 0, stream>>>(RX, WA2p, RY);
+    k_dftB<17,34,9,2720,256><<<374, 256, 0, stream>>>(RY, Wn2p, Wg2p, RX);
+    k_dftC<17,9,34,2720,256><<<99, 256, 0, stream>>>(RX, WC2p, xt3, slOff, 5440);
+  }
+  k_coef_t<9,34,9,256><<<cdiv_h(160*Q9,256), 256, 0, stream>>>(xt3, dAT3p, xh3, Q9, 160, 5440);
+  k_yh_t<<<cdiv_h(Q9*384,256), 256, 0, stream>>>(xh3, kh3, yh3t, 9, 5, 12, Q9);
+
+  k_synth3<9,18,5,9,64,384><<<384*18, 64, 0, stream>>>(yh3t, dS3p, tw18p, xt4);
+  k_coef<<<cdiv_h(384*Q5,256), 256, 0, stream>>>(xt4, dA4p, xh4, 5, 18, 5, 9, Q5, 384);
+  k_yh_t<<<cdiv_h(Q5*896,256), 256, 0, stream>>>(xh4, kh4, yh4t, 5, 12, 28, Q5);
+
+  k_synth2<5,10,3,5,0,1,64,896><<<896*10, 64, 0, stream>>>(yh4t, dS4p, tw10p, Wn4p, Wg4p, xt5, nullptr, nullptr);
+  k_coef<<<cdiv_h(896*Q3,256), 256, 0, stream>>>(xt5, dA5p, xh5, 3, 10, 3, 5, Q3, 896);
+  k_yh_t<<<cdiv_h(Q3*2048,256), 256, 0, stream>>>(xh5, kh5, yh5t, 3, 28, 64, Q3);
+
+  k_synth2<3,6,3,5,1,1,64,2048><<<2048*6, 64, 0, stream>>>(yh5t, dS5p, tw6p, Wn5p, nullptr, nullptr, s5p, wIntp);
 
   k_mlp<<<1, 256, 0, stream>>>(s5p, g1, be1, w1, b1, g2, be2, w2, b2, g3, be3, w3, b3, out);
 }
```

Measured after the change: 1.075 ms. 1.15x slower.
